# Kernel tuning notes

Measured on AMD Instinct MI355X. Metric: run time of the kernel, lower is better.

## Reference

```python
import jax, jax.numpy as jnp
import numpy as np
from jax import lax

H, P, N, G, K, CHUNK = 64, 64, 128, 1, 4, 256
D_MODEL = 2048
D_INNER = H * P            # 4096
CONV_DIM = D_INNER + 2 * G * N  # 4352
EPS = 1e-5


def setup_inputs() -> dict:
    key = jax.random.key(0)
    ks = jax.random.split(key, 6)
    s = lambda k, shape, scale: jax.random.normal(k, shape, jnp.float32) * scale
    return {
        "hidden_states": s(ks[0], (2, 2048, D_MODEL), 1.0),
        "in_proj_w": s(ks[1], (D_MODEL, D_INNER + CONV_DIM + H), D_MODEL ** -0.5),
        "conv_w": s(ks[2], (CONV_DIM, K), K ** -0.5),
        "conv_b": jnp.zeros((CONV_DIM,), jnp.float32),
        "dt_bias": jnp.ones((H,), jnp.float32),
        "A_log": jnp.log(jnp.arange(1, H + 1, dtype=jnp.float32)),
        "D_param": jnp.ones((H,), jnp.float32),
        "norm_w": jnp.ones((D_INNER,), jnp.float32),
        "out_proj_w": s(ks[3], (D_INNER, D_MODEL), D_INNER ** -0.5),
    }


def _mamba2_forward(hidden_states, in_proj_w, conv_w, conv_b, dt_bias, A_log, D_param, norm_w, out_proj_w):
    b, l, _ = hidden_states.shape
    c = l // CHUNK  # number of chunks

    # in_proj -> gate | conv channels (x,B,C) | dt
    proj = hidden_states @ in_proj_w
    gate = proj[..., :D_INNER]
    hbc = proj[..., D_INNER:D_INNER + CONV_DIM]
    dt = proj[..., D_INNER + CONV_DIM:]  # [b,l,H]

    # depthwise causal conv1d + silu
    xt = hbc.transpose(0, 2, 1)  # [b, CONV_DIM, l]
    y = lax.conv_general_dilated(
        xt, conv_w[:, None, :], window_strides=(1,), padding=[(K - 1, 0)],
        feature_group_count=CONV_DIM, dimension_numbers=("NCH", "OIH", "NCH"))
    hbc = jax.nn.silu(y + conv_b[None, :, None]).transpose(0, 2, 1)  # [b,l,CONV_DIM]

    # split into x / B / C per group (unflatten over groups as in torch code)
    per_g = D_INNER // G
    hg = hbc.reshape(b, l, G, per_g + 2 * N)
    x = hg[..., :per_g].reshape(b, l, H, P)                 # [b,l,h,p]
    Bm = hg[..., per_g:per_g + N]                            # [b,l,g,n]
    Cm = hg[..., per_g + N:]                                 # [b,l,g,n]
    hpg = H // G
    Bh = jnp.repeat(Bm, hpg, axis=2)                         # [b,l,h,n]
    Ch = jnp.repeat(Cm, hpg, axis=2)

    # dt: softplus(dt + bias), clamp per time_step_limit (0, inf)
    dt = jax.nn.softplus(dt + dt_bias)                       # [b,l,h]
    A = -jnp.exp(A_log)                                      # [h]

    # chunk the sequence
    x_c = x.reshape(b, c, CHUNK, H, P)
    B_c = Bh.reshape(b, c, CHUNK, H, N)
    C_c = Ch.reshape(b, c, CHUNK, H, N)
    dt_c = dt.reshape(b, c, CHUNK, H)

    dA = dt_c * A[None, None, None, :]                       # [b,c,L,h]
    cum = jnp.cumsum(dA, axis=2)                             # [b,c,L,h]

    # intra-chunk (diagonal block): decay[i,j] = exp(cum_i - cum_j), i>=j
    diff = cum[:, :, :, None, :] - cum[:, :, None, :, :]     # [b,c,i,j,h]
    i = jnp.arange(CHUNK)
    mask = i[:, None] >= i[None, :]
    decay = jnp.exp(jnp.where(mask[None, None, :, :, None], diff, -jnp.inf))
    scores = jnp.einsum("bcihn,bcjhn->bcijh", C_c, B_c) * decay * dt_c[:, :, None, :, :]
    Y_diag = jnp.einsum("bcijh,bcjhp->bcihp", scores, x_c)   # [b,c,L,h,p]

    # per-chunk final states
    decay_states = jnp.exp(cum[:, :, -1:, :] - cum)          # [b,c,L,h]
    states = jnp.einsum("bclh,bclhn,bclhp->bchpn", decay_states * dt_c, B_c, x_c)
    chunk_decay = jnp.exp(cum[:, :, -1, :])                  # [b,c,h]

    # inter-chunk recurrence over chunks
    def step(prev, inp):
        st, cd = inp  # [b,h,p,n], [b,h]
        new = cd[:, :, None, None] * prev + st
        return new, prev

    init = jnp.zeros((b, H, P, N), hidden_states.dtype)
    _, prev_states = lax.scan(step, init, (jnp.moveaxis(states, 1, 0), jnp.moveaxis(chunk_decay, 1, 0)))
    prev_states = jnp.moveaxis(prev_states, 0, 1)            # [b,c,h,p,n]

    state_decay_out = jnp.exp(cum)                           # [b,c,L,h]
    Y_off = jnp.einsum("bclhn,bchpn,bclh->bclhp", C_c, prev_states, state_decay_out)

    yh = (Y_diag + Y_off).reshape(b, l, H, P) + D_param[None, None, :, None] * x
    yr = yh.reshape(b, l, D_INNER)

    # gated RMSNorm
    hidden = yr * jax.nn.silu(gate)
    var = jnp.mean(hidden * hidden, axis=-1, keepdims=True)
    hidden = hidden * lax.rsqrt(var + EPS) * norm_w

    return hidden @ out_proj_w


def reference(hidden_states, in_proj_w, conv_w, conv_b, dt_bias, A_log, D_param, norm_w, out_proj_w):
    return _mamba2_forward(hidden_states, in_proj_w, conv_w, conv_b, dt_bias, A_log, D_param, norm_w, out_proj_w)
```

## Files before the change

kernel.cpp:

```cpp
#include <hip/hip_runtime.h>
#include <hip/hip_bf16.h>


typedef __attribute__((ext_vector_type(8))) _Float16 f16x8;
typedef __attribute__((ext_vector_type(4))) float f32x4;

#define GLD16(gp, lp) __builtin_amdgcn_global_load_lds( \
    (__attribute__((address_space(1))) void*)(gp),      \
    (__attribute__((address_space(3))) void*)(lp), 16, 0, 0)

__device__ __forceinline__ unsigned short f2h(float v) {
  _Float16 h = (_Float16)v;
  return *reinterpret_cast<unsigned short*>(&h);
}
__device__ __forceinline__ float h2f(unsigned short u) {
  _Float16 h = *reinterpret_cast<_Float16*>(&u);
  return (float)h;
}
__device__ __forceinline__ float siluf(float x) { return x / (1.f + expf(-x)); }

__global__ __launch_bounds__(256) void cast_f16(const float* __restrict__ s,
                                                _Float16* __restrict__ d) {
  long i = ((long)blockIdx.x * 256 + threadIdx.x) * 4;
  float4 v = *reinterpret_cast<const float4*>(s + i);
  ushort4 u;
  u.x = f2h(v.x); u.y = f2h(v.y); u.z = f2h(v.z); u.w = f2h(v.w);
  *reinterpret_cast<ushort4*>(d + i) = u;
}

__global__ __launch_bounds__(256) void transpose_win(const float* __restrict__ src,
                                                     _Float16* __restrict__ dst) {
  __shared__ float tile[32][33];
  int c0 = blockIdx.x * 32, r0 = blockIdx.y * 32;
  int tx = threadIdx.x, ty = threadIdx.y;
#pragma unroll
  for (int i = 0; i < 4; i++)
    tile[ty + i * 8][tx] = src[(long)(r0 + ty + i * 8) * 8512 + c0 + tx];
  __syncthreads();
#pragma unroll
  for (int i = 0; i < 4; i++) {
    int c = c0 + ty + i * 8, r = r0 + tx;
    dst[(long)c * 2048 + r] = (_Float16)tile[tx][ty + i * 8];
  }
}

__global__ __launch_bounds__(256) void transpose_wout(const float* __restrict__ src,
                                                      _Float16* __restrict__ dst,
                                                      int R, int C) {
  __shared__ float tile[32][33];
  int c0 = blockIdx.x * 32, r0 = blockIdx.y * 32;
  int tx = threadIdx.x, ty = threadIdx.y;
#pragma unroll
  for (int i = 0; i < 4; i++)
    tile[ty + i * 8][tx] = src[(long)(r0 + ty + i * 8) * C + c0 + tx];
  __syncthreads();
#pragma unroll
  for (int i = 0; i < 4; i++) {
    int c = c0 + ty + i * 8, r = r0 + tx;
    dst[(long)c * R + r] = (_Float16)tile[tx][ty + i * 8];
  }
}

__global__ __launch_bounds__(512, 2) void gemm_in8(const _Float16* __restrict__ A,
                                                   const _Float16* __restrict__ Bt,
                                                   _Float16* __restrict__ gate,
                                                   float* __restrict__ hbcf,
                                                   float* __restrict__ rparts) {
  __shared__ __attribute__((aligned(128))) char ldsB[131072];
  const int tid = threadIdx.x;
  const int lane = tid & 63;
  const int wv = tid >> 6;
  const int wr = wv >> 2, wc = wv & 3;
  const int wg = blockIdx.x;
  const bool rem = wg >= 512;
  int by, bxn, kbase, zz;
  if (!rem) {
    const int swz = (wg & 7) * 64 + (wg >> 3);
    by = swz >> 5; bxn = swz & 31; kbase = 0; zz = 0;
  } else {
    const int idx = wg - 512;
    by = idx & 15; zz = idx >> 4; bxn = 32; kbase = zz * 256;
  }

  const int srow = tid >> 3;
  const int scolg = (tid & 7) ^ (srow & 7);
  const _Float16* Ab = A + (long)by * 524288 + (long)srow * 2048 + scolg * 8 + kbase;
  const _Float16* Bb = Bt + (long)bxn * 524288 + (long)srow * 2048 + scolg * 8 + kbase;
  const int ldst = tid << 4;

#define STAGE_A(tau, h) do {                                              \
    const _Float16* g_ = Ab + (long)(h) * 262144 + (tau) * 64;            \
    char* l_ = ldsB + ((((tau) & 1) << 2) + (h)) * 16384 + ldst;          \
    GLD16(g_, l_); GLD16(g_ + 131072, l_ + 8192); } while (0)
#define STAGE_B(tau, h) do {                                              \
    const _Float16* g_ = Bb + (long)(h) * 262144 + (tau) * 64;            \
    char* l_ = ldsB + ((((tau) & 1) << 2) + 2 + (h)) * 16384 + ldst;      \
    GLD16(g_, l_); GLD16(g_ + 131072, l_ + 8192); } while (0)

  const int fr = lane & 15;
  const int c16 = (lane >> 4) ^ (fr & 7);
  const int aOff = wr * 16384 + fr * 128 + c16 * 16;
  const int bOff = (2 + (wc >> 1)) * 16384 + ((wc & 1) * 64 + fr) * 128 + c16 * 16;
#define RD_A(b, mi, k32) (*(const f16x8*)(ldsB + ((aOff + (b) * 65536 + (mi) * 2048) ^ ((k32) * 64))))
#define RD_B(b, ni, k32) (*(const f16x8*)(ldsB + ((bOff + (b) * 65536 + (ni) * 2048) ^ ((k32) * 64))))

#define BAR() __builtin_amdgcn_s_barrier()
#define WLG0() asm volatile("s_waitcnt lgkmcnt(0)" ::: "memory")
#define WLG8() asm volatile("s_waitcnt lgkmcnt(8)" ::: "memory")
#define WVM4() asm volatile("s_waitcnt vmcnt(4)" ::: "memory")

  f32x4 acc[8][4];
#pragma unroll
  for (int mi = 0; mi < 8; ++mi)
#pragma unroll
    for (int ni = 0; ni < 4; ++ni) acc[mi][ni] = f32x4{0.f, 0.f, 0.f, 0.f};

  STAGE_A(0, 0); STAGE_A(0, 1); STAGE_B(0, 0); STAGE_B(0, 1);
  STAGE_B(1, 0); STAGE_B(1, 1);
  WVM4(); BAR();

#define MFMA_Q(MI0, MI1, x0, x1, x2, x3, PB)                                        \
  __builtin_amdgcn_s_setprio(1);                                                    \
  _Pragma("unroll") for (int ni = 0; ni < 4; ++ni) {                                \
    acc[MI0][ni] = __builtin_amdgcn_mfma_f32_16x16x32_f16(x0, PB[ni][0], acc[MI0][ni], 0, 0, 0); \
    acc[MI0][ni] = __builtin_amdgcn_mfma_f32_16x16x32_f16(x1, PB[ni][1], acc[MI0][ni], 0, 0, 0); \
    acc[MI1][ni] = __builtin_amdgcn_mfma_f32_16x16x32_f16(x2, PB[ni][0], acc[MI1][ni], 0, 0, 0); \
    acc[MI1][ni] = __builtin_amdgcn_mfma_f32_16x16x32_f16(x3, PB[ni][1], acc[MI1][ni], 0, 0, 0); \
  }                                                                                 \
  __builtin_amdgcn_s_setprio(0);

#define ITER8(u, msk) do {                                                          \
    const int t1 = (2 * (u) + 1) & (msk);                                           \
    const int t2 = (2 * (u) + 2) & (msk);                                           \
    const int t3 = (2 * (u) + 3) & (msk);                                           \
    f16x8 PB0[4][2];                                                                \
    _Pragma("unroll") for (int ni = 0; ni < 4; ++ni) {                              \
      PB0[ni][0] = RD_B(0, ni, 0); PB0[ni][1] = RD_B(0, ni, 1); }                   \
    {                                                                               \
      f16x8 x0 = RD_A(0, 0, 0), x1 = RD_A(0, 0, 1), x2 = RD_A(0, 1, 0), x3 = RD_A(0, 1, 1); \
      STAGE_A(t1, 0); WLG8(); BAR(); WLG0();                                        \
      MFMA_Q(0, 1, x0, x1, x2, x3, PB0) BAR();                                      \
    }                                                                               \
    {                                                                               \
      f16x8 x0 = RD_A(0, 2, 0), x1 = RD_A(0, 2, 1), x2 = RD_A(0, 3, 0), x3 = RD_A(0, 3, 1); \
      STAGE_A(t1, 1); BAR(); WLG0();                                                \
      MFMA_Q(2, 3, x0, x1, x2, x3, PB0) BAR();                                      \
    }                                                                               \
    {                                                                               \
      f16x8 x0 = RD_A(0, 4, 0), x1 = RD_A(0, 4, 1), x2 = RD_A(0, 5, 0), x3 = RD_A(0, 5, 1); \
      STAGE_B(t2, 0); BAR(); WLG0();                                                \
      MFMA_Q(4, 5, x0, x1, x2, x3, PB0) BAR();                                      \
    }                                                                               \
    {                                                                               \
      f16x8 x0 = RD_A(0, 6, 0), x1 = RD_A(0, 6, 1), x2 = RD_A(0, 7, 0), x3 = RD_A(0, 7, 1); \
      STAGE_B(t2, 1); BAR(); WLG0();                                                \
      MFMA_Q(6, 7, x0, x1, x2, x3, PB0) WVM4(); BAR();                              \
    }                                                                               \
    f16x8 PB1[4][2];                                                                \
    _Pragma("unroll") for (int ni = 0; ni < 4; ++ni) {                              \
      PB1[ni][0] = RD_B(1, ni, 0); PB1[ni][1] = RD_B(1, ni, 1); }                   \
    {                                                                               \
      f16x8 x0 = RD_A(1, 0, 0), x1 = RD_A(1, 0, 1), x2 = RD_A(1, 1, 0), x3 = RD_A(1, 1, 1); \
      STAGE_A(t2, 0); WLG8(); BAR(); WLG0();                                        \
      MFMA_Q(0, 1, x0, x1, x2, x3, PB1) BAR();                                      \
    }                                                                               \
    {                                                                               \
      f16x8 x0 = RD_A(1, 2, 0), x1 = RD_A(1, 2, 1), x2 = RD_A(1, 3, 0), x3 = RD_A(1, 3, 1); \
      STAGE_A(t2, 1); BAR(); WLG0();                                                \
      MFMA_Q(2, 3, x0, x1, x2, x3, PB1) BAR();                                      \
    }                                                                               \
    {                                                                               \
      f16x8 x0 = RD_A(1, 4, 0), x1 = RD_A(1, 4, 1), x2 = RD_A(1, 5, 0), x3 = RD_A(1, 5, 1); \
      STAGE_B(t3, 0); BAR(); WLG0();                                                \
      MFMA_Q(4, 5, x0, x1, x2, x3, PB1) BAR();                                      \
    }                                                                               \
    {                                                                               \
      f16x8 x0 = RD_A(1, 6, 0), x1 = RD_A(1, 6, 1), x2 = RD_A(1, 7, 0), x3 = RD_A(1, 7, 1); \
      STAGE_B(t3, 1); BAR(); WLG0();                                                \
      MFMA_Q(6, 7, x0, x1, x2, x3, PB1) WVM4(); BAR();                              \
    }                                                                               \
  } while (0)

  if (!rem) {
    for (int u = 0; u < 16; ++u) ITER8(u, 31);
  } else {
    for (int u = 0; u < 2; ++u) ITER8(u, 3);
  }

  const int m0 = by * 256 + wr * 128;
  const int cl = lane & 15, rq = (lane >> 4) * 4;
  if (!rem) {
    const int n0 = bxn * 256 + wc * 64;
    if (bxn < 16) {
#pragma unroll
      for (int mi = 0; mi < 8; ++mi)
#pragma unroll
        for (int r = 0; r < 4; ++r) {
          long rowoff = (long)(m0 + mi * 16 + rq + r) * 4096 + n0 + cl;
#pragma unroll
          for (int ni = 0; ni < 4; ++ni) gate[rowoff + ni * 16] = (_Float16)acc[mi][ni][r];
        }
    } else {
#pragma unroll
      for (int mi = 0; mi < 8; ++mi)
#pragma unroll
        for (int r = 0; r < 4; ++r) {
          long rowoff = (long)(m0 + mi * 16 + rq + r) * 4352 + (n0 - 4096) + cl;
#pragma unroll
          for (int ni = 0; ni < 4; ++ni) hbcf[rowoff + ni * 16] = acc[mi][ni][r];
        }
    }
  } else {
    float* rp = rparts + (long)zz * 1048576;
    const int ncol = wc * 64;
#pragma unroll
    for (int mi = 0; mi < 8; ++mi)
#pragma unroll
      for (int r = 0; r < 4; ++r) {
        long rowoff = (long)(m0 + mi * 16 + rq + r) * 256 + ncol + cl;
#pragma unroll
        for (int ni = 0; ni < 4; ++ni) rp[rowoff + ni * 16] = acc[mi][ni][r];
      }
  }
#undef STAGE_A
#undef STAGE_B
#undef RD_A
#undef RD_B
#undef ITER8
}

__global__ __launch_bounds__(256) void add_rem(const float* __restrict__ rp,
                                               float* __restrict__ hbcf) {
  long e = ((long)blockIdx.x * 256 + threadIdx.x) * 4;
  float4 s = *reinterpret_cast<const float4*>(rp + e);
#pragma unroll
  for (int z = 1; z < 8; ++z) {
    float4 v = *reinterpret_cast<const float4*>(rp + (long)z * 1048576 + e);
    s.x += v.x; s.y += v.y; s.z += v.z; s.w += v.w;
  }
  long row = e >> 8, col = e & 255;
  *reinterpret_cast<float4*>(hbcf + row * 4352 + 4096 + col) = s;
}

__global__ __launch_bounds__(512, 2) void gemm_out8(const _Float16* __restrict__ A,
                                                    const _Float16* __restrict__ Bt,
                                                    float* __restrict__ Cp) {
  __shared__ __attribute__((aligned(128))) char ldsB[131072];
  const int tid = threadIdx.x;
  const int lane = tid & 63;
  const int wv = tid >> 6;
  const int wr = wv >> 2, wc = wv & 3;
  const int wg = blockIdx.x;
  const int z = wg >> 7;
  const int r7 = wg & 127;
  const int sw = (r7 & 7) * 16 + (r7 >> 3);
  const int by = sw >> 3, bx = sw & 7;

  const int srow = tid >> 3;
  const int scolg = (tid & 7) ^ (srow & 7);
  const _Float16* Ab = A + (long)by * 256 * 4096 + (long)z * 2048 +
                       (long)srow * 4096 + scolg * 8;
  const _Float16* Bb = Bt + (long)bx * 256 * 4096 + (long)z * 2048 +
                       (long)srow * 4096 + scolg * 8;
  const int ldst = tid << 4;

#define STAGE_A(tau, h) do {                                              \
    const _Float16* g_ = Ab + (long)(h) * 524288 + (tau) * 64;            \
    char* l_ = ldsB + ((((tau) & 1) << 2) + (h)) * 16384 + ldst;          \
    GLD16(g_, l_); GLD16(g_ + 262144, l_ + 8192); } while (0)
#define STAGE_B(tau, h) do {                                              \
    const _Float16* g_ = Bb + (long)(h) * 524288 + (tau) * 64;            \
    char* l_ = ldsB + ((((tau) & 1) << 2) + 2 + (h)) * 16384 + ldst;      \
    GLD16(g_, l_); GLD16(g_ + 262144, l_ + 8192); } while (0)

  const int fr = lane & 15;
  const int c16 = (lane >> 4) ^ (fr & 7);
  const int aOff = wr * 16384 + fr * 128 + c16 * 16;
  const int bOff = (2 + (wc >> 1)) * 16384 + ((wc & 1) * 64 + fr) * 128 + c16 * 16;
#define RD_A(b, mi, k32) (*(const f16x8*)(ldsB + ((aOff + (b) * 65536 + (mi) * 2048) ^ ((k32) * 64))))
#define RD_B(b, ni, k32) (*(const f16x8*)(ldsB + ((bOff + (b) * 65536 + (ni) * 2048) ^ ((k32) * 64))))

  f32x4 acc[8][4];
#pragma unroll
  for (int mi = 0; mi < 8; ++mi)
#pragma unroll
    for (int ni = 0; ni < 4; ++ni) acc[mi][ni] = f32x4{0.f, 0.f, 0.f, 0.f};

  STAGE_A(0, 0); STAGE_A(0, 1); STAGE_B(0, 0); STAGE_B(0, 1);
  STAGE_B(1, 0); STAGE_B(1, 1);
  WVM4(); BAR();

  for (int u = 0; u < 16; ++u) {
    const int t1 = 2 * u + 1;
    const int t2 = (2 * u + 2) & 31;
    const int t3 = (2 * u + 3) & 31;
    f16x8 PB0[4][2];
#pragma unroll
    for (int ni = 0; ni < 4; ++ni) { PB0[ni][0] = RD_B(0, ni, 0); PB0[ni][1] = RD_B(0, ni, 1); }
    {
      f16x8 x0 = RD_A(0, 0, 0), x1 = RD_A(0, 0, 1), x2 = RD_A(0, 1, 0), x3 = RD_A(0, 1, 1);
      STAGE_A(t1, 0); WLG8(); BAR(); WLG0();
      MFMA_Q(0, 1, x0, x1, x2, x3, PB0) BAR();
    }
    {
      f16x8 x0 = RD_A(0, 2, 0), x1 = RD_A(0, 2, 1), x2 = RD_A(0, 3, 0), x3 = RD_A(0, 3, 1);
      STAGE_A(t1, 1); BAR(); WLG0();
      MFMA_Q(2, 3, x0, x1, x2, x3, PB0) BAR();
    }
    {
      f16x8 x0 = RD_A(0, 4, 0), x1 = RD_A(0, 4, 1), x2 = RD_A(0, 5, 0), x3 = RD_A(0, 5, 1);
      STAGE_B(t2, 0); BAR(); WLG0();
      MFMA_Q(4, 5, x0, x1, x2, x3, PB0) BAR();
    }
    {
      f16x8 x0 = RD_A(0, 6, 0), x1 = RD_A(0, 6, 1), x2 = RD_A(0, 7, 0), x3 = RD_A(0, 7, 1);
      STAGE_B(t2, 1); BAR(); WLG0();
      MFMA_Q(6, 7, x0, x1, x2, x3, PB0) WVM4(); BAR();
    }
    f16x8 PB1[4][2];
#pragma unroll
    for (int ni = 0; ni < 4; ++ni) { PB1[ni][0] = RD_B(1, ni, 0); PB1[ni][1] = RD_B(1, ni, 1); }
    {
      f16x8 x0 = RD_A(1, 0, 0), x1 = RD_A(1, 0, 1), x2 = RD_A(1, 1, 0), x3 = RD_A(1, 1, 1);
      STAGE_A(t2, 0); WLG8(); BAR(); WLG0();
      MFMA_Q(0, 1, x0, x1, x2, x3, PB1) BAR();
    }
    {
      f16x8 x0 = RD_A(1, 2, 0), x1 = RD_A(1, 2, 1), x2 = RD_A(1, 3, 0), x3 = RD_A(1, 3, 1);
      STAGE_A(t2, 1); BAR(); WLG0();
      MFMA_Q(2, 3, x0, x1, x2, x3, PB1) BAR();
    }
    {
      f16x8 x0 = RD_A(1, 4, 0), x1 = RD_A(1, 4, 1), x2 = RD_A(1, 5, 0), x3 = RD_A(1, 5, 1);
      STAGE_B(t3, 0); BAR(); WLG0();
      MFMA_Q(4, 5, x0, x1, x2, x3, PB1) BAR();
    }
    {
      f16x8 x0 = RD_A(1, 6, 0), x1 = RD_A(1, 6, 1), x2 = RD_A(1, 7, 0), x3 = RD_A(1, 7, 1);
      STAGE_B(t3, 1); BAR(); WLG0();
      MFMA_Q(6, 7, x0, x1, x2, x3, PB1) WVM4(); BAR();
    }
  }
  const int m0 = by * 256 + wr * 128;
  const int n0 = bx * 256 + wc * 64;
  const int cl = lane & 15, rq = (lane >> 4) * 4;
  float* Cb = Cp + (long)z * 8388608;
#pragma unroll
  for (int mi = 0; mi < 8; ++mi)
#pragma unroll
    for (int r = 0; r < 4; ++r) {
      long rowoff = (long)(m0 + mi * 16 + rq + r) * 2048 + n0 + cl;
#pragma unroll
      for (int ni = 0; ni < 4; ++ni) Cb[rowoff + ni * 16] = acc[mi][ni][r];
    }
#undef STAGE_A
#undef STAGE_B
#undef RD_A
#undef RD_B
#undef BAR
#undef WLG0
#undef WLG8
#undef WVM4
#undef MFMA_Q
}

__global__ __launch_bounds__(256) void add_out(const float* __restrict__ p,
                                               float* __restrict__ o) {
  long i = ((long)blockIdx.x * 256 + threadIdx.x) * 4;
  float4 a = *reinterpret_cast<const float4*>(p + i);
  float4 b = *reinterpret_cast<const float4*>(p + 8388608 + i);
  float4 r;
  r.x = a.x + b.x; r.y = a.y + b.y; r.z = a.z + b.z; r.w = a.w + b.w;
  *reinterpret_cast<float4*>(o + i) = r;
}

__global__ __launch_bounds__(256) void gemm_bt(const _Float16* __restrict__ A,
                                               const _Float16* __restrict__ Bt,
                                               float* __restrict__ Cf,
                                               int K, int ldc,
                                               long zsA, long zsB, long zsC) {
  __shared__ uint4 As4[512];
  __shared__ uint4 Bs4[512];
  _Float16* As = (_Float16*)As4;
  _Float16* Bs = (_Float16*)Bs4;
  const int tid = threadIdx.x;
  const int wv = tid >> 6;
  const int lane = tid & 63;
  const _Float16* Ab = A + (long)blockIdx.z * zsA + (long)blockIdx.y * 128 * K;
  const _Float16* Bb = Bt + (long)blockIdx.z * zsB + (long)blockIdx.x * 128 * K;
  const int c0 = wv * 128 + lane;
  const int c1 = c0 + 64;
  const long ra0 = (long)(c0 >> 2) * K + (c0 & 3) * 8;
  const long ra1 = (long)(c1 >> 2) * K + (c1 & 3) * 8;
  f32x4 acc[4][4];
#pragma unroll
  for (int mi = 0; mi < 4; mi++)
#pragma unroll
    for (int ni = 0; ni < 4; ni++) acc[mi][ni] = f32x4{0.f, 0.f, 0.f, 0.f};
  const int mrow = (wv & 1) * 64 + (lane & 15);
  const int nrow = (wv >> 1) * 64 + (lane & 15);
  const int koff = (lane >> 4) * 8;
  for (int k0 = 0; k0 < K; k0 += 32) {
    GLD16(Ab + ra0 + k0, (char*)As + c0 * 16);
    GLD16(Ab + ra1 + k0, (char*)As + c1 * 16);
    GLD16(Bb + ra0 + k0, (char*)Bs + c0 * 16);
    GLD16(Bb + ra1 + k0, (char*)Bs + c1 * 16);
    __syncthreads();
    f16x8 af[4], bfr[4];
#pragma unroll
    for (int mi = 0; mi < 4; mi++)
      af[mi] = *(const f16x8*)(As + (mrow + mi * 16) * 32 + koff);
#pragma unroll
    for (int ni = 0; ni < 4; ni++)
      bfr[ni] = *(const f16x8*)(Bs + (nrow + ni * 16) * 32 + koff);
#pragma unroll
    for (int mi = 0; mi < 4; mi++)
#pragma unroll
      for (int ni = 0; ni < 4; ni++)
        acc[mi][ni] = __builtin_amdgcn_mfma_f32_16x16x32_f16(af[mi], bfr[ni],
                                                             acc[mi][ni], 0, 0, 0);
    __syncthreads();
  }
  const int m0 = blockIdx.y * 128 + (wv & 1) * 64;
  const int n0 = blockIdx.x * 128 + (wv >> 1) * 64;
  const int cl = lane & 15, rq = (lane >> 4) * 4;
  const long zc = (long)blockIdx.z * zsC;
#pragma unroll
  for (int mi = 0; mi < 4; mi++)
#pragma unroll
    for (int r = 0; r < 4; r++) {
      long rowoff = zc + (long)(m0 + mi * 16 + rq + r) * ldc + n0 + cl;
#pragma unroll
      for (int ni = 0; ni < 4; ni++) Cf[rowoff + ni * 16] = acc[mi][ni][r];
    }
}

__global__ __launch_bounds__(256) void dtz_kernel(const float* __restrict__ hs,
                                                  const float* __restrict__ Win,
                                                  float* __restrict__ zf) {
  __shared__ float Xs[4][2048];
  int t0 = blockIdx.x * 4;
  int tid = threadIdx.x;
#pragma unroll
  for (int i = 0; i < 8; i++) {
    int e = tid * 4 + i * 1024;
    int tok = e >> 11, k = e & 2047;
    *reinterpret_cast<float4*>(&Xs[tok][k]) =
        *reinterpret_cast<const float4*>(&hs[(long)(t0 + tok) * 2048 + k]);
  }
  __syncthreads();
  int h = tid & 63, tg = tid >> 6;
  float a0 = 0.f, a1 = 0.f, a2 = 0.f, a3 = 0.f;
  const float* wcol = Win + 8448 + h;
  for (int k = 0; k < 2048; k += 4) {
    a0 = fmaf(Xs[tg][k + 0], wcol[(long)(k + 0) * 8512], a0);
    a1 = fmaf(Xs[tg][k + 1], wcol[(long)(k + 1) * 8512], a1);
    a2 = fmaf(Xs[tg][k + 2], wcol[(long)(k + 2) * 8512], a2);
    a3 = fmaf(Xs[tg][k + 3], wcol[(long)(k + 3) * 8512], a3);
  }
  zf[(long)(t0 + tg) * 64 + h] = (a0 + a1) + (a2 + a3);
}

__global__ __launch_bounds__(256) void conv_silu_kernel(const float* __restrict__ hbcf,
                                                        const float* __restrict__ convw,
                                                        const float* __restrict__ convb,
                                                        _Float16* __restrict__ x16,
                                                        _Float16* __restrict__ B16,
                                                        _Float16* __restrict__ C16) {
  int q = blockIdx.x * 256 + threadIdx.x;
  int t = blockIdx.y;
  int l = t & 2047;
  const float* col = hbcf + (long)t * 4352 + q;
  float4 wq = *reinterpret_cast<const float4*>(convw + q * 4);
  float a = convb[q];
  if (l >= 3) a += col[-3 * 4352] * wq.x;
  if (l >= 2) a += col[-2 * 4352] * wq.y;
  if (l >= 1) a += col[-1 * 4352] * wq.z;
  a += col[0] * wq.w;
  _Float16 o = (_Float16)siluf(a);
  if (q < 4096) x16[(long)t * 4096 + q] = o;
  else if (q < 4224) B16[(long)t * 128 + (q - 4096)] = o;
  else C16[(long)t * 128 + (q - 4224)] = o;
}

__global__ __launch_bounds__(256) void xtrans(const unsigned short* __restrict__ src,
                                              unsigned short* __restrict__ dst) {
  __shared__ unsigned short tile[64][66];
  int c0 = blockIdx.x * 64, r0 = blockIdx.y * 64;
  int tx = threadIdx.x & 15, ty = threadIdx.x >> 4;
#pragma unroll
  for (int i = 0; i < 4; i++) {
    int r = ty + i * 16;
    ushort4 v = *(const ushort4*)&src[(long)(r0 + r) * 4096 + c0 + 4 * tx];
    tile[r][4 * tx] = v.x; tile[r][4 * tx + 1] = v.y;
    tile[r][4 * tx + 2] = v.z; tile[r][4 * tx + 3] = v.w;
  }
  __syncthreads();
#pragma unroll
  for (int i = 0; i < 4; i++) {
    int c = ty + i * 16;
    ushort4 v;
    v.x = tile[4 * tx + 0][c]; v.y = tile[4 * tx + 1][c];
    v.z = tile[4 * tx + 2][c]; v.w = tile[4 * tx + 3][c];
    *(ushort4*)&dst[(long)(c0 + c) * 4096 + r0 + 4 * tx] = v;
  }
}

__global__ __launch_bounds__(256) void dt_cum_kernel(const float* __restrict__ zf,
                                                     const float* __restrict__ dtb,
                                                     const float* __restrict__ Alog,
                                                     float* __restrict__ dt_f,
                                                     float* __restrict__ cum_f,
                                                     float* __restrict__ cuml) {
  int bc = blockIdx.x;
  int h = threadIdx.x & 63, seg = threadIdx.x >> 6;
  int t0 = bc * 256;
  float Ah = -expf(Alog[h]);
  float bias = dtb[h];
  __shared__ float segsum[4][64];
  float s = 0.f;
  for (int j = 0; j < 64; j++) {
    int t = t0 + seg * 64 + j;
    float z = zf[(long)t * 64 + h] + bias;
    float v = (z > 20.f) ? z : log1pf(expf(z));
    dt_f[(long)t * 64 + h] = v;
    s += v * Ah;
  }
  segsum[seg][h] = s;
  __syncthreads();
  float run = 0.f;
  for (int k = 0; k < seg; k++) run += segsum[k][h];
  for (int j = 0; j < 64; j++) {
    int t = t0 + seg * 64 + j;
    run += dt_f[(long)t * 64 + h] * Ah;
    cum_f[(long)t * 64 + h] = run;
  }
  if (seg == 3) cuml[bc * 64 + h] = run;
}

__global__ __launch_bounds__(256) void states_mfma(const unsigned short* __restrict__ xT16,
                                                   const unsigned short* __restrict__ B16,
                                                   const float* __restrict__ dt_f,
                                                   const float* __restrict__ cum_f,
                                                   const float* __restrict__ cuml,
                                                   float* __restrict__ states) {
  int h = blockIdx.x, bc = blockIdx.y;
  int t0 = bc * 256, tid = threadIdx.x;
  __shared__ float w_s[256];
  __shared__ unsigned short Aw[64 * 40];
  __shared__ unsigned short BT[128 * 40];
  {
    int t = t0 + tid;
    w_s[tid] = expf(cuml[bc * 64 + h] - cum_f[(long)t * 64 + h]) * dt_f[(long)t * 64 + h];
  }
  __syncthreads();
  int wv = tid >> 6, lane = tid & 63;
  int mr = lane & 15, koff = (lane >> 4) * 8;
  f32x4 acc[4][2];
#pragma unroll
  for (int mi = 0; mi < 4; mi++)
#pragma unroll
    for (int nj = 0; nj < 2; nj++) acc[mi][nj] = f32x4{0.f, 0.f, 0.f, 0.f};
  for (int kt = 0; kt < 8; kt++) {
    {
      int p = tid >> 2, tq = tid & 3;
      const unsigned short* g = &xT16[((long)(h * 64 + p)) * 4096 + t0 + kt * 32 + tq * 8];
      ushort4 u0 = *(const ushort4*)g, u1 = *(const ushort4*)(g + 4);
      const float* wp = &w_s[kt * 32 + tq * 8];
      ushort4 o0, o1;
      o0.x = f2h(h2f(u0.x) * wp[0]); o0.y = f2h(h2f(u0.y) * wp[1]);
      o0.z = f2h(h2f(u0.z) * wp[2]); o0.w = f2h(h2f(u0.w) * wp[3]);
      o1.x = f2h(h2f(u1.x) * wp[4]); o1.y = f2h(h2f(u1.y) * wp[5]);
      o1.z = f2h(h2f(u1.z) * wp[6]); o1.w = f2h(h2f(u1.w) * wp[7]);
      *(ushort4*)&Aw[p * 40 + tq * 8] = o0;
      *(ushort4*)&Aw[p * 40 + tq * 8 + 4] = o1;
    }
    {
      int tl = tid >> 3, ng = tid & 7;
      const unsigned short* g = &B16[((long)(t0 + kt * 32 + tl)) * 128 + ng * 16];
#pragma unroll
      for (int j = 0; j < 16; j++) BT[(ng * 16 + j) * 40 + tl] = g[j];
    }
    __syncthreads();
    f16x8 af[4], bf[2];
#pragma unroll
    for (int mi = 0; mi < 4; mi++)
      af[mi] = *(const f16x8*)&Aw[(mi * 16 + mr) * 40 + koff];
#pragma unroll
    for (int nj = 0; nj < 2; nj++)
      bf[nj] = *(const f16x8*)&BT[((wv * 2 + nj) * 16 + mr) * 40 + koff];
#pragma unroll
    for (int mi = 0; mi < 4; mi++)
#pragma unroll
      for (int nj = 0; nj < 2; nj++)
        acc[mi][nj] = __builtin_amdgcn_mfma_f32_16x16x32_f16(af[mi], bf[nj],
                                                             acc[mi][nj], 0, 0, 0);
    __syncthreads();
  }
  int cl = lane & 15, rq = (lane >> 4) * 4;
  long base = ((long)(bc * 64 + h)) * 8192;
#pragma unroll
  for (int mi = 0; mi < 4; mi++)
#pragma unroll
    for (int r = 0; r < 4; r++) {
      int p = mi * 16 + rq + r;
#pragma unroll
      for (int nj = 0; nj < 2; nj++) {
        int n = (wv * 2 + nj) * 16 + cl;
        states[base + p * 128 + n] = acc[mi][nj][r];
      }
    }
}

__global__ __launch_bounds__(256) void recur_kernel(float* __restrict__ states,
                                                    const float* __restrict__ cuml) {
  int bh = blockIdx.x;
  int b = bh >> 6, h = bh & 63;
  int tid = threadIdx.x;
  float4 prev[8];
#pragma unroll
  for (int j = 0; j < 8; j++) prev[j] = make_float4(0.f, 0.f, 0.f, 0.f);
  for (int c = 0; c < 8; c++) {
    int bc = b * 8 + c;
    float cd = expf(cuml[bc * 64 + h]);
    long base = (long)(bc * 64 + h) * 8192;
#pragma unroll
    for (int j = 0; j < 8; j++) {
      long o = base + j * 1024 + tid * 4;
      float4 st = *reinterpret_cast<const float4*>(&states[o]);
      *reinterpret_cast<float4*>(&states[o]) = prev[j];
      prev[j].x = fmaf(cd, prev[j].x, st.x);
      prev[j].y = fmaf(cd, prev[j].y, st.y);
      prev[j].z = fmaf(cd, prev[j].z, st.z);
      prev[j].w = fmaf(cd, prev[j].w, st.w);
    }
  }
}

__global__ __launch_bounds__(256) void yfused(const unsigned short* __restrict__ xT16,
                                              const unsigned short* __restrict__ x16,
                                              const unsigned short* __restrict__ C16,
                                              const float* __restrict__ CBT,
                                              const float* __restrict__ states,
                                              const float* __restrict__ dt_f,
                                              const float* __restrict__ cum_f,
                                              const float* __restrict__ Dp,
                                              float* __restrict__ Ysum) {
  int h = blockIdx.x, bc = blockIdx.y;
  int t0 = bc * 256, tid = threadIdx.x;
  __shared__ unsigned short Sb[256 * 40];
  __shared__ unsigned short Xb[64 * 264];
  __shared__ float cum_s[256], dt_s[256];
  int i = tid;
  cum_s[i] = cum_f[(long)(t0 + i) * 64 + h];
  dt_s[i] = dt_f[(long)(t0 + i) * 64 + h];
  {
    int p = tid >> 2, tq = tid & 3;
    const unsigned short* g = &xT16[((long)(h * 64 + p)) * 4096 + t0 + tq * 64];
    unsigned short* l = &Xb[p * 264 + tq * 64];
#pragma unroll
    for (int c = 0; c < 8; c++)
      *(uint4*)(l + c * 8) = *(const uint4*)(g + c * 8);
  }
  __syncthreads();
  float cum_i = cum_s[i];
  const float* cbrow = CBT + (long)bc * 65536 + (long)i * 256;
  int wv = tid >> 6, lane = tid & 63;
  int mr = lane & 15, koff = (lane >> 4) * 8;
  f32x4 acc[4][4];
#pragma unroll
  for (int mi = 0; mi < 4; mi++)
#pragma unroll
    for (int ni = 0; ni < 4; ni++) acc[mi][ni] = f32x4{0.f, 0.f, 0.f, 0.f};
  for (int kt = 0; kt < 8; kt++) {
    int k0 = kt * 32;
#pragma unroll
    for (int c = 0; c < 8; c++) {
      float4 cb = *(const float4*)&cbrow[k0 + c * 4];
      ushort4 o;
      {
        int j = k0 + c * 4 + 0;
        float s = (j <= i) ? cb.x * expf(cum_i - cum_s[j]) * dt_s[j] : 0.f;
        o.x = f2h(s);
      }
      {
        int j = k0 + c * 4 + 1;
        float s = (j <= i) ? cb.y * expf(cum_i - cum_s[j]) * dt_s[j] : 0.f;
        o.y = f2h(s);
      }
      {
        int j = k0 + c * 4 + 2;
        float s = (j <= i) ? cb.z * expf(cum_i - cum_s[j]) * dt_s[j] : 0.f;
        o.z = f2h(s);
      }
      {
        int j = k0 + c * 4 + 3;
        float s = (j <= i) ? cb.w * expf(cum_i - cum_s[j]) * dt_s[j] : 0.f;
        o.w = f2h(s);
      }
      *(ushort4*)&Sb[i * 40 + c * 4] = o;
    }
    __syncthreads();
    if (kt <= 2 * wv + 1) {
      f16x8 af[4], bf[4];
#pragma unroll
      for (int mi = 0; mi < 4; mi++)
        af[mi] = *(const f16x8*)&Sb[(64 * wv + mi * 16 + mr) * 40 + koff];
#pragma unroll
      for (int ni = 0; ni < 4; ni++)
        bf[ni] = *(const f16x8*)&Xb[(ni * 16 + mr) * 264 + k0 + koff];
#pragma unroll
      for (int mi = 0; mi < 4; mi++)
#pragma unroll
        for (int ni = 0; ni < 4; ni++)
          acc[mi][ni] = __builtin_amdgcn_mfma_f32_16x16x32_f16(af[mi], bf[ni],
                                                               acc[mi][ni], 0, 0, 0);
    }
    __syncthreads();
  }
  {
    int p = tid >> 2, nq = tid & 3;
    const float* g = &states[((long)(bc * 64 + h)) * 8192 + p * 128 + nq * 32];
    unsigned short* l = &Xb[p * 136 + nq * 32];
#pragma unroll
    for (int c = 0; c < 8; c++) {
      float4 v = *(const float4*)(g + c * 4);
      ushort4 u;
      u.x = f2h(v.x); u.y = f2h(v.y); u.z = f2h(v.z); u.w = f2h(v.w);
      *(ushort4*)(l + c * 4) = u;
    }
  }
  float fac_i = expf(cum_i);
  for (int kn = 0; kn < 4; kn++) {
    {
      const unsigned short* g = &C16[((long)(t0 + i)) * 128 + kn * 32];
#pragma unroll
      for (int c = 0; c < 8; c++) {
        ushort4 u = *(const ushort4*)(g + c * 4);
        ushort4 o;
        o.x = f2h(h2f(u.x) * fac_i); o.y = f2h(h2f(u.y) * fac_i);
        o.z = f2h(h2f(u.z) * fac_i); o.w = f2h(h2f(u.w) * fac_i);
        *(ushort4*)&Sb[i * 40 + c * 4] = o;
      }
    }
    __syncthreads();
    f16x8 af[4], bf[4];
#pragma unroll
    for (int mi = 0; mi < 4; mi++)
      af[mi] = *(const f16x8*)&Sb[(64 * wv + mi * 16 + mr) * 40 + koff];
#pragma unroll
    for (int ni = 0; ni < 4; ni++)
      bf[ni] = *(const f16x8*)&Xb[(ni * 16 + mr) * 136 + kn * 32 + koff];
#pragma unroll
    for (int mi = 0; mi < 4; mi++)
#pragma unroll
      for (int ni = 0; ni < 4; ni++)
        acc[mi][ni] = __builtin_amdgcn_mfma_f32_16x16x32_f16(af[mi], bf[ni],
                                                             acc[mi][ni], 0, 0, 0);
    __syncthreads();
  }
  float Dh = Dp[h];
  int cl = lane & 15, rq = (lane >> 4) * 4;
#pragma unroll
  for (int mi = 0; mi < 4; mi++)
#pragma unroll
    for (int r = 0; r < 4; r++) {
      long row = t0 + 64 * wv + mi * 16 + rq + r;
      float* yr = &Ysum[row * 4096 + h * 64];
      const unsigned short* xr = &x16[row * 4096 + h * 64];
#pragma unroll
      for (int ni = 0; ni < 4; ni++) {
        int p = ni * 16 + cl;
        yr[p] = acc[mi][ni][r] + Dh * h2f(xr[p]);
      }
    }
}

__global__ __launch_bounds__(256) void norm_kernel(const float* __restrict__ Ysum,
                                                   const _Float16* __restrict__ gate,
                                                   const float* __restrict__ nw,
                                                   _Float16* __restrict__ hid) {
  int t = blockIdx.x;
  int tid = threadIdx.x;
  float hv[16];
  float ss = 0.f;
#pragma unroll
  for (int k = 0; k < 4; k++) {
    int d = tid * 4 + k * 1024;
    float4 y = *reinterpret_cast<const float4*>(&Ysum[(long)t * 4096 + d]);
    ushort4 gu = *reinterpret_cast<const ushort4*>(gate + (long)t * 4096 + d);
    float h0 = y.x * siluf(h2f(gu.x)), h1 = y.y * siluf(h2f(gu.y));
    float h2 = y.z * siluf(h2f(gu.z)), h3 = y.w * siluf(h2f(gu.w));
    hv[k * 4 + 0] = h0; hv[k * 4 + 1] = h1; hv[k * 4 + 2] = h2; hv[k * 4 + 3] = h3;
    ss += h0 * h0 + h1 * h1 + h2 * h2 + h3 * h3;
  }
#pragma unroll
  for (int o = 32; o > 0; o >>= 1) ss += __shfl_down(ss, o, 64);
  __shared__ float ws4[4];
  if ((tid & 63) == 0) ws4[tid >> 6] = ss;
  __syncthreads();
  float var = (ws4[0] + ws4[1] + ws4[2] + ws4[3]) * (1.f / 4096.f);
  float scale = rsqrtf(var + 1e-5f);
#pragma unroll
  for (int k = 0; k < 4; k++) {
    int d = tid * 4 + k * 1024;
    ushort4 u;
#pragma unroll
    for (int c = 0; c < 4; c++)
      ((unsigned short*)&u)[c] = f2h(hv[k * 4 + c] * scale * nw[d + c]);
    *reinterpret_cast<ushort4*>(hid + (long)t * 4096 + d) = u;
  }
}

extern "C" void kernel_launch(void* const* d_in, const int* in_sizes, int n_in,
                              void* d_out, int out_size, void* d_ws, size_t ws_size,
                              hipStream_t stream) {
  (void)in_sizes; (void)n_in; (void)out_size; (void)ws_size;
  const float* hs    = (const float*)d_in[0];
  const float* Win   = (const float*)d_in[1];
  const float* convw = (const float*)d_in[2];
  const float* convb = (const float*)d_in[3];
  const float* dtb   = (const float*)d_in[4];
  const float* Alog  = (const float*)d_in[5];
  const float* Dp    = (const float*)d_in[6];
  const float* nw    = (const float*)d_in[7];
  const float* Wout  = (const float*)d_in[8];
  float* out = (float*)d_out;

  char* base = (char*)d_ws;
  size_t off = 0;
  auto take = [&](size_t n) { char* r = base + off; off += (n + 255) & ~(size_t)255; return r; };
  float*    hbcf  = (float*)take(4096UL * 4352 * 4);
  _Float16* gateh = (_Float16*)take(4096UL * 4096 * 2);
  _Float16* Ah    = (_Float16*)take(4096UL * 2048 * 2);
  _Float16* WtH   = (_Float16*)take(8448UL * 2048 * 2);
  _Float16* xT16  = (_Float16*)take(4096UL * 4096 * 2);
  _Float16* B16   = (_Float16*)take(4096UL * 128 * 2);
  _Float16* C16   = (_Float16*)take(4096UL * 128 * 2);
  float*    zf    = (float*)take(4096UL * 64 * 4);
  float*    dt_f  = (float*)take(4096UL * 64 * 4);
  float*    cum_f = (float*)take(4096UL * 64 * 4);
  float*    cuml  = (float*)take(16UL * 64 * 4);
  float*    CBT   = (float*)take(16UL * 256 * 256 * 4);
  float*    states= (float*)take(1024UL * 8192 * 4);
  float*    Ysum  = hbcf;
  float*    oparts= hbcf;
  float*    rparts= states;
  _Float16* WoutT = Ah;
  _Float16* x16   = WtH;
  _Float16* hid   = (_Float16*)states;

  dim3 tb(32, 8);
  cast_f16<<<8192, 256, 0, stream>>>(hs, Ah);
  transpose_win<<<dim3(264, 64), tb, 0, stream>>>(Win, WtH);
  dtz_kernel<<<1024, 256, 0, stream>>>(hs, Win, zf);
  gemm_in8<<<dim3(640), 512, 0, stream>>>(Ah, WtH, gateh, hbcf, rparts);
  add_rem<<<1024, 256, 0, stream>>>(rparts, hbcf);
  transpose_wout<<<dim3(64, 128), tb, 0, stream>>>(Wout, WoutT, 4096, 2048);
  conv_silu_kernel<<<dim3(17, 4096), 256, 0, stream>>>(hbcf, convw, convb, x16, B16, C16);
  dt_cum_kernel<<<16, 256, 0, stream>>>(zf, dtb, Alog, dt_f, cum_f, cuml);
  xtrans<<<dim3(64, 64), 256, 0, stream>>>((const unsigned short*)x16, (unsigned short*)xT16);
  gemm_bt<<<dim3(2, 2, 16), 256, 0, stream>>>(C16, B16, CBT, 128, 256,
                                              32768, 32768, 65536);
  states_mfma<<<dim3(64, 16), 256, 0, stream>>>((const unsigned short*)xT16,
                                                (const unsigned short*)B16,
                                                dt_f, cum_f, cuml, states);
  recur_kernel<<<128, 256, 0, stream>>>(states, cuml);
  yfused<<<dim3(64, 16), 256, 0, stream>>>((const unsigned short*)xT16,
                                           (const unsigned short*)x16,
                                           (const unsigned short*)C16,
                                           CBT, states, dt_f, cum_f, Dp, Ysum);
  norm_kernel<<<4096, 256, 0, stream>>>(Ysum, gateh, nw, hid);
  gemm_out8<<<dim3(256), 512, 0, stream>>>(hid, WoutT, oparts);
  add_out<<<8192, 256, 0, stream>>>(oparts, out);
}
```

Measured before the change: 777.3 us.

## Merge independent small kernels into multi-role launches and fuse conv with transpose

Independent preprocessing kernels are merged into single launches that branch on block index: cast, dt projection and W_in transpose become one prep kernel; dt cumsum, split-K reduction and W_out transpose become fuse2; the states and CB GEMMs become fuse3. The conv+silu kernel now also writes the transposed x tile directly, removing the separate xtrans pass. This cuts launch overhead and lets small tasks run concurrently, at the cost of heterogeneous blocks sharing one launch configuration and shared-memory size.

```diff
diff --git a/kernel.cpp b/kernel.cpp
--- a/kernel.cpp
+++ b/kernel.cpp
@@ -19,45 +19,55 @@
 }
 __device__ __forceinline__ float siluf(float x) { return x / (1.f + expf(-x)); }
 
-__global__ __launch_bounds__(256) void cast_f16(const float* __restrict__ s,
-                                                _Float16* __restrict__ d) {
-  long i = ((long)blockIdx.x * 256 + threadIdx.x) * 4;
-  float4 v = *reinterpret_cast<const float4*>(s + i);
-  ushort4 u;
-  u.x = f2h(v.x); u.y = f2h(v.y); u.z = f2h(v.z); u.w = f2h(v.w);
-  *reinterpret_cast<ushort4*>(d + i) = u;
-}
-
-__global__ __launch_bounds__(256) void transpose_win(const float* __restrict__ src,
-                                                     _Float16* __restrict__ dst) {
-  __shared__ float tile[32][33];
-  int c0 = blockIdx.x * 32, r0 = blockIdx.y * 32;
-  int tx = threadIdx.x, ty = threadIdx.y;
-#pragma unroll
-  for (int i = 0; i < 4; i++)
-    tile[ty + i * 8][tx] = src[(long)(r0 + ty + i * 8) * 8512 + c0 + tx];
-  __syncthreads();
-#pragma unroll
-  for (int i = 0; i < 4; i++) {
-    int c = c0 + ty + i * 8, r = r0 + tx;
-    dst[(long)c * 2048 + r] = (_Float16)tile[tx][ty + i * 8];
-  }
-}
-
-__global__ __launch_bounds__(256) void transpose_wout(const float* __restrict__ src,
-                                                      _Float16* __restrict__ dst,
-                                                      int R, int C) {
-  __shared__ float tile[32][33];
-  int c0 = blockIdx.x * 32, r0 = blockIdx.y * 32;
-  int tx = threadIdx.x, ty = threadIdx.y;
-#pragma unroll
-  for (int i = 0; i < 4; i++)
-    tile[ty + i * 8][tx] = src[(long)(r0 + ty + i * 8) * C + c0 + tx];
-  __syncthreads();
-#pragma unroll
-  for (int i = 0; i < 4; i++) {
-    int c = c0 + ty + i * 8, r = r0 + tx;
-    dst[(long)c * R + r] = (_Float16)tile[tx][ty + i * 8];
+__global__ __launch_bounds__(256) void prep(const float* __restrict__ hs,
+                                            const float* __restrict__ Win,
+                                            _Float16* __restrict__ Ah,
+                                            _Float16* __restrict__ WtH,
+                                            float* __restrict__ zf) {
+  __shared__ __attribute__((aligned(16))) char smemP[32768];
+  const int bid = blockIdx.x;
+  const int tid = threadIdx.x;
+  if (bid < 1024) {
+    float (*Xs)[2048] = reinterpret_cast<float (*)[2048]>(smemP);
+    int t0 = bid * 4;
+#pragma unroll
+    for (int i = 0; i < 8; i++) {
+      int e = tid * 4 + i * 1024;
+      int tok = e >> 11, k = e & 2047;
+      *reinterpret_cast<float4*>(&Xs[tok][k]) =
+          *reinterpret_cast<const float4*>(&hs[(long)(t0 + tok) * 2048 + k]);
+    }
+    __syncthreads();
+    int h = tid & 63, tg = tid >> 6;
+    float a0 = 0.f, a1 = 0.f, a2 = 0.f, a3 = 0.f;
+    const float* wcol = Win + 8448 + h;
+    for (int k = 0; k < 2048; k += 4) {
+      a0 = fmaf(Xs[tg][k + 0], wcol[(long)(k + 0) * 8512], a0);
+      a1 = fmaf(Xs[tg][k + 1], wcol[(long)(k + 1) * 8512], a1);
+      a2 = fmaf(Xs[tg][k + 2], wcol[(long)(k + 2) * 8512], a2);
+      a3 = fmaf(Xs[tg][k + 3], wcol[(long)(k + 3) * 8512], a3);
+    }
+    zf[(long)(t0 + tg) * 64 + h] = (a0 + a1) + (a2 + a3);
+  } else if (bid < 9216) {
+    long i = ((long)(bid - 1024) * 256 + tid) * 4;
+    float4 v = *reinterpret_cast<const float4*>(hs + i);
+    ushort4 u;
+    u.x = f2h(v.x); u.y = f2h(v.y); u.z = f2h(v.z); u.w = f2h(v.w);
+    *reinterpret_cast<ushort4*>((unsigned short*)Ah + i) = u;
+  } else {
+    float (*tile)[33] = reinterpret_cast<float (*)[33]>(smemP);
+    int i = bid - 9216;
+    int c0 = (i % 264) * 32, r0 = (i / 264) * 32;
+    int tx = tid & 31, ty = tid >> 5;
+#pragma unroll
+    for (int j = 0; j < 4; j++)
+      tile[ty + j * 8][tx] = Win[(long)(r0 + ty + j * 8) * 8512 + c0 + tx];
+    __syncthreads();
+#pragma unroll
+    for (int j = 0; j < 4; j++) {
+      int c = c0 + ty + j * 8, r = r0 + tx;
+      WtH[(long)c * 2048 + r] = (_Float16)tile[tx][ty + j * 8];
+    }
   }
 }
 
@@ -229,387 +239,258 @@
 #undef ITER8
 }
 
-__global__ __launch_bounds__(256) void add_rem(const float* __restrict__ rp,
-                                               float* __restrict__ hbcf) {
-  long e = ((long)blockIdx.x * 256 + threadIdx.x) * 4;
-  float4 s = *reinterpret_cast<const float4*>(rp + e);
-#pragma unroll
-  for (int z = 1; z < 8; ++z) {
-    float4 v = *reinterpret_cast<const float4*>(rp + (long)z * 1048576 + e);
-    s.x += v.x; s.y += v.y; s.z += v.z; s.w += v.w;
-  }
-  long row = e >> 8, col = e & 255;
-  *reinterpret_cast<float4*>(hbcf + row * 4352 + 4096 + col) = s;
-}
-
-__global__ __launch_bounds__(512, 2) void gemm_out8(const _Float16* __restrict__ A,
-                                                    const _Float16* __restrict__ Bt,
-                                                    float* __restrict__ Cp) {
-  __shared__ __attribute__((aligned(128))) char ldsB[131072];
+__global__ __launch_bounds__(256) void fuse2(const float* __restrict__ zf,
+                                             const float* __restrict__ dtb,
+                                             const float* __restrict__ Alog,
+                                             float* __restrict__ dt_f,
+                                             float* __restrict__ cum_f,
+                                             float* __restrict__ cuml,
+                                             const float* __restrict__ rp,
+                                             float* __restrict__ hbcf,
+                                             const float* __restrict__ Wout,
+                                             _Float16* __restrict__ WoutT) {
+  __shared__ __attribute__((aligned(16))) char smem2[4352];
+  const int bid = blockIdx.x;
   const int tid = threadIdx.x;
-  const int lane = tid & 63;
-  const int wv = tid >> 6;
-  const int wr = wv >> 2, wc = wv & 3;
-  const int wg = blockIdx.x;
-  const int z = wg >> 7;
-  const int r7 = wg & 127;
-  const int sw = (r7 & 7) * 16 + (r7 >> 3);
-  const int by = sw >> 3, bx = sw & 7;
-
-  const int srow = tid >> 3;
-  const int scolg = (tid & 7) ^ (srow & 7);
-  const _Float16* Ab = A + (long)by * 256 * 4096 + (long)z * 2048 +
-                       (long)srow * 4096 + scolg * 8;
-  const _Float16* Bb = Bt + (long)bx * 256 * 4096 + (long)z * 2048 +
-                       (long)srow * 4096 + scolg * 8;
-  const int ldst = tid << 4;
-
-#define STAGE_A(tau, h) do {                                              \
-    const _Float16* g_ = Ab + (long)(h) * 524288 + (tau) * 64;            \
-    char* l_ = ldsB + ((((tau) & 1) << 2) + (h)) * 16384 + ldst;          \
-    GLD16(g_, l_); GLD16(g_ + 262144, l_ + 8192); } while (0)
-#define STAGE_B(tau, h) do {                                              \
-    const _Float16* g_ = Bb + (long)(h) * 524288 + (tau) * 64;            \
-    char* l_ = ldsB + ((((tau) & 1) << 2) + 2 + (h)) * 16384 + ldst;      \
-    GLD16(g_, l_); GLD16(g_ + 262144, l_ + 8192); } while (0)
-
-  const int fr = lane & 15;
-  const int c16 = (lane >> 4) ^ (fr & 7);
-  const int aOff = wr * 16384 + fr * 128 + c16 * 16;
-  const int bOff = (2 + (wc >> 1)) * 16384 + ((wc & 1) * 64 + fr) * 128 + c16 * 16;
-#define RD_A(b, mi, k32) (*(const f16x8*)(ldsB + ((aOff + (b) * 65536 + (mi) * 2048) ^ ((k32) * 64))))
-#define RD_B(b, ni, k32) (*(const f16x8*)(ldsB + ((bOff + (b) * 65536 + (ni) * 2048) ^ ((k32) * 64))))
-
-  f32x4 acc[8][4];
-#pragma unroll
-  for (int mi = 0; mi < 8; ++mi)
-#pragma unroll
-    for (int ni = 0; ni < 4; ++ni) acc[mi][ni] = f32x4{0.f, 0.f, 0.f, 0.f};
-
-  STAGE_A(0, 0); STAGE_A(0, 1); STAGE_B(0, 0); STAGE_B(0, 1);
-  STAGE_B(1, 0); STAGE_B(1, 1);
-  WVM4(); BAR();
-
-  for (int u = 0; u < 16; ++u) {
-    const int t1 = 2 * u + 1;
-    const int t2 = (2 * u + 2) & 31;
-    const int t3 = (2 * u + 3) & 31;
-    f16x8 PB0[4][2];
-#pragma unroll
-    for (int ni = 0; ni < 4; ++ni) { PB0[ni][0] = RD_B(0, ni, 0); PB0[ni][1] = RD_B(0, ni, 1); }
-    {
-      f16x8 x0 = RD_A(0, 0, 0), x1 = RD_A(0, 0, 1), x2 = RD_A(0, 1, 0), x3 = RD_A(0, 1, 1);
-      STAGE_A(t1, 0); WLG8(); BAR(); WLG0();
-      MFMA_Q(0, 1, x0, x1, x2, x3, PB0) BAR();
-    }
-    {
-      f16x8 x0 = RD_A(0, 2, 0), x1 = RD_A(0, 2, 1), x2 = RD_A(0, 3, 0), x3 = RD_A(0, 3, 1);
-      STAGE_A(t1, 1); BAR(); WLG0();
-      MFMA_Q(2, 3, x0, x1, x2, x3, PB0) BAR();
-    }
-    {
-      f16x8 x0 = RD_A(0, 4, 0), x1 = RD_A(0, 4, 1), x2 = RD_A(0, 5, 0), x3 = RD_A(0, 5, 1);
-      STAGE_B(t2, 0); BAR(); WLG0();
-      MFMA_Q(4, 5, x0, x1, x2, x3, PB0) BAR();
-    }
-    {
-      f16x8 x0 = RD_A(0, 6, 0), x1 = RD_A(0, 6, 1), x2 = RD_A(0, 7, 0), x3 = RD_A(0, 7, 1);
-      STAGE_B(t2, 1); BAR(); WLG0();
-      MFMA_Q(6, 7, x0, x1, x2, x3, PB0) WVM4(); BAR();
-    }
-    f16x8 PB1[4][2];
-#pragma unroll
-    for (int ni = 0; ni < 4; ++ni) { PB1[ni][0] = RD_B(1, ni, 0); PB1[ni][1] = RD_B(1, ni, 1); }
-    {
-      f16x8 x0 = RD_A(1, 0, 0), x1 = RD_A(1, 0, 1), x2 = RD_A(1, 1, 0), x3 = RD_A(1, 1, 1);
-      STAGE_A(t2, 0); WLG8(); BAR(); WLG0();
-      MFMA_Q(0, 1, x0, x1, x2, x3, PB1) BAR();
-    }
-    {
-      f16x8 x0 = RD_A(1, 2, 0), x1 = RD_A(1, 2, 1), x2 = RD_A(1, 3, 0), x3 = RD_A(1, 3, 1);
-      STAGE_A(t2, 1); BAR(); WLG0();
-      MFMA_Q(2, 3, x0, x1, x2, x3, PB1) BAR();
-    }
-    {
-      f16x8 x0 = RD_A(1, 4, 0), x1 = RD_A(1, 4, 1), x2 = RD_A(1, 5, 0), x3 = RD_A(1, 5, 1);
-      STAGE_B(t3, 0); BAR(); WLG0();
-      MFMA_Q(4, 5, x0, x1, x2, x3, PB1) BAR();
-    }
-    {
-      f16x8 x0 = RD_A(1, 6, 0), x1 = RD_A(1, 6, 1), x2 = RD_A(1, 7, 0), x3 = RD_A(1, 7, 1);
-      STAGE_B(t3, 1); BAR(); WLG0();
-      MFMA_Q(6, 7, x0, x1, x2, x3, PB1) WVM4(); BAR();
-    }
-  }
-  const int m0 = by * 256 + wr * 128;
-  const int n0 = bx * 256 + wc * 64;
-  const int cl = lane & 15, rq = (lane >> 4) * 4;
-  float* Cb = Cp + (long)z * 8388608;
-#pragma unroll
-  for (int mi = 0; mi < 8; ++mi)
-#pragma unroll
-    for (int r = 0; r < 4; ++r) {
-      long rowoff = (long)(m0 + mi * 16 + rq + r) * 2048 + n0 + cl;
-#pragma unroll
-      for (int ni = 0; ni < 4; ++ni) Cb[rowoff + ni * 16] = acc[mi][ni][r];
-    }
-#undef STAGE_A
-#undef STAGE_B
-#undef RD_A
-#undef RD_B
-#undef BAR
-#undef WLG0
-#undef WLG8
-#undef WVM4
-#undef MFMA_Q
-}
-
-__global__ __launch_bounds__(256) void add_out(const float* __restrict__ p,
-                                               float* __restrict__ o) {
-  long i = ((long)blockIdx.x * 256 + threadIdx.x) * 4;
-  float4 a = *reinterpret_cast<const float4*>(p + i);
-  float4 b = *reinterpret_cast<const float4*>(p + 8388608 + i);
-  float4 r;
-  r.x = a.x + b.x; r.y = a.y + b.y; r.z = a.z + b.z; r.w = a.w + b.w;
-  *reinterpret_cast<float4*>(o + i) = r;
-}
-
-__global__ __launch_bounds__(256) void gemm_bt(const _Float16* __restrict__ A,
-                                               const _Float16* __restrict__ Bt,
-                                               float* __restrict__ Cf,
-                                               int K, int ldc,
-                                               long zsA, long zsB, long zsC) {
-  __shared__ uint4 As4[512];
-  __shared__ uint4 Bs4[512];
-  _Float16* As = (_Float16*)As4;
-  _Float16* Bs = (_Float16*)Bs4;
+  if (bid < 16) {
+    float (*segsum)[64] = reinterpret_cast<float (*)[64]>(smem2);
+    int bc = bid;
+    int h = tid & 63, seg = tid >> 6;
+    int t0 = bc * 256;
+    float Ah = -expf(Alog[h]);
+    float bias = dtb[h];
+    float s = 0.f;
+    for (int j = 0; j < 64; j++) {
+      int t = t0 + seg * 64 + j;
+      float z = zf[(long)t * 64 + h] + bias;
+      float v = (z > 20.f) ? z : log1pf(expf(z));
+      dt_f[(long)t * 64 + h] = v;
+      s += v * Ah;
+    }
+    segsum[seg][h] = s;
+    __syncthreads();
+    float run = 0.f;
+    for (int k = 0; k < seg; k++) run += segsum[k][h];
+    for (int j = 0; j < 64; j++) {
+      int t = t0 + seg * 64 + j;
+      run += dt_f[(long)t * 64 + h] * Ah;
+      cum_f[(long)t * 64 + h] = run;
+    }
+    if (seg == 3) cuml[bc * 64 + h] = run;
+  } else if (bid < 1040) {
+    long e = ((long)(bid - 16) * 256 + tid) * 4;
+    float4 s = *reinterpret_cast<const float4*>(rp + e);
+#pragma unroll
+    for (int z = 1; z < 8; ++z) {
+      float4 v = *reinterpret_cast<const float4*>(rp + (long)z * 1048576 + e);
+      s.x += v.x; s.y += v.y; s.z += v.z; s.w += v.w;
+    }
+    long row = e >> 8, col = e & 255;
+    *reinterpret_cast<float4*>(hbcf + row * 4352 + 4096 + col) = s;
+  } else {
+    float (*tile)[33] = reinterpret_cast<float (*)[33]>(smem2);
+    int i = bid - 1040;
+    int c0 = (i & 63) * 32, r0 = (i >> 6) * 32;
+    int tx = tid & 31, ty = tid >> 5;
+#pragma unroll
+    for (int j = 0; j < 4; j++)
+      tile[ty + j * 8][tx] = Wout[(long)(r0 + ty + j * 8) * 2048 + c0 + tx];
+    __syncthreads();
+#pragma unroll
+    for (int j = 0; j < 4; j++) {
+      int c = c0 + ty + j * 8, r = r0 + tx;
+      WoutT[(long)c * 4096 + r] = (_Float16)tile[tx][ty + j * 8];
+    }
+  }
+}
+
+__global__ __launch_bounds__(256) void convx(const float* __restrict__ hbcf,
+                                             const float* __restrict__ convw,
+                                             const float* __restrict__ convb,
+                                             _Float16* __restrict__ x16,
+                                             _Float16* __restrict__ B16,
+                                             _Float16* __restrict__ C16,
+                                             unsigned short* __restrict__ xT16) {
+  __shared__ unsigned short tile[64][66];
+  const int bx = blockIdx.x, t0 = blockIdx.y * 64;
   const int tid = threadIdx.x;
-  const int wv = tid >> 6;
-  const int lane = tid & 63;
-  const _Float16* Ab = A + (long)blockIdx.z * zsA + (long)blockIdx.y * 128 * K;
-  const _Float16* Bb = Bt + (long)blockIdx.z * zsB + (long)blockIdx.x * 128 * K;
-  const int c0 = wv * 128 + lane;
-  const int c1 = c0 + 64;
-  const long ra0 = (long)(c0 >> 2) * K + (c0 & 3) * 8;
-  const long ra1 = (long)(c1 >> 2) * K + (c1 & 3) * 8;
-  f32x4 acc[4][4];
-#pragma unroll
-  for (int mi = 0; mi < 4; mi++)
-#pragma unroll
-    for (int ni = 0; ni < 4; ni++) acc[mi][ni] = f32x4{0.f, 0.f, 0.f, 0.f};
-  const int mrow = (wv & 1) * 64 + (lane & 15);
-  const int nrow = (wv >> 1) * 64 + (lane & 15);
-  const int koff = (lane >> 4) * 8;
-  for (int k0 = 0; k0 < K; k0 += 32) {
-    GLD16(Ab + ra0 + k0, (char*)As + c0 * 16);
-    GLD16(Ab + ra1 + k0, (char*)As + c1 * 16);
-    GLD16(Bb + ra0 + k0, (char*)Bs + c0 * 16);
-    GLD16(Bb + ra1 + k0, (char*)Bs + c1 * 16);
-    __syncthreads();
-    f16x8 af[4], bfr[4];
+  const int tq = tid & 63, tg = tid >> 6;
+  const int q0 = (bx < 64) ? bx * 64 : 4096 + (bx - 64) * 64;
+  const int q = q0 + tq;
+  const int ts = t0 + tg * 16;
+  const int bstart = ts & ~2047;
+  const float* colq = hbcf + q;
+  float4 wq = *reinterpret_cast<const float4*>(convw + q * 4);
+  float bconv = convb[q];
+  float v3 = (ts - 3 >= bstart) ? colq[(long)(ts - 3) * 4352] : 0.f;
+  float v2 = (ts - 2 >= bstart) ? colq[(long)(ts - 2) * 4352] : 0.f;
+  float v1 = (ts - 1 >= bstart) ? colq[(long)(ts - 1) * 4352] : 0.f;
+  if (bx < 64) {
+#pragma unroll
+    for (int j = 0; j < 16; ++j) {
+      int t = ts + j;
+      float v0 = colq[(long)t * 4352];
+      float a = bconv + v3 * wq.x + v2 * wq.y + v1 * wq.z + v0 * wq.w;
+      unsigned short o = f2h(siluf(a));
+      ((unsigned short*)x16)[(long)t * 4096 + q] = o;
+      tile[tg * 16 + j][tq] = o;
+      v3 = v2; v2 = v1; v1 = v0;
+    }
+    __syncthreads();
+    int tx = tid & 15, ty = tid >> 4;
+#pragma unroll
+    for (int i = 0; i < 4; ++i) {
+      int c = ty + i * 16;
+      ushort4 v;
+      v.x = tile[4 * tx + 0][c]; v.y = tile[4 * tx + 1][c];
+      v.z = tile[4 * tx + 2][c]; v.w = tile[4 * tx + 3][c];
+      *(ushort4*)&xT16[(long)(q0 + c) * 4096 + t0 + 4 * tx] = v;
+    }
+  } else {
+#pragma unroll
+    for (int j = 0; j < 16; ++j) {
+      int t = ts + j;
+      float v0 = colq[(long)t * 4352];
+      float a = bconv + v3 * wq.x + v2 * wq.y + v1 * wq.z + v0 * wq.w;
+      _Float16 o = (_Float16)siluf(a);
+      if (q < 4224) B16[(long)t * 128 + (q - 4096)] = o;
+      else C16[(long)t * 128 + (q - 4224)] = o;
+      v3 = v2; v2 = v1; v1 = v0;
+    }
+  }
+}
+
+__global__ __launch_bounds__(256) void fuse3(const unsigned short* __restrict__ xT16,
+                                             const _Float16* __restrict__ B16,
+                                             const _Float16* __restrict__ C16,
+                                             const float* __restrict__ dt_f,
+                                             const float* __restrict__ cum_f,
+                                             const float* __restrict__ cuml,
+                                             float* __restrict__ states,
+                                             float* __restrict__ CBT) {
+  __shared__ __attribute__((aligned(16))) char smem3[16384];
+  const int bid = blockIdx.x;
+  const int tid = threadIdx.x;
+  const int wv = tid >> 6, lane = tid & 63;
+  const int mr = lane & 15, koff = (lane >> 4) * 8;
+  if (bid < 1024) {
+    float* w_s = (float*)smem3;
+    unsigned short* Aw = (unsigned short*)(smem3 + 1024);
+    unsigned short* BT = (unsigned short*)(smem3 + 6144);
+    int h = bid & 63, bc = bid >> 6;
+    int t0 = bc * 256;
+    {
+      int t = t0 + tid;
+      w_s[tid] = expf(cuml[bc * 64 + h] - cum_f[(long)t * 64 + h]) * dt_f[(long)t * 64 + h];
+    }
+    __syncthreads();
+    f32x4 acc[4][2];
 #pragma unroll
     for (int mi = 0; mi < 4; mi++)
-      af[mi] = *(const f16x8*)(As + (mrow + mi * 16) * 32 + koff);
-#pragma unroll
-    for (int ni = 0; ni < 4; ni++)
-      bfr[ni] = *(const f16x8*)(Bs + (nrow + ni * 16) * 32 + koff);
+#pragma unroll
+      for (int nj = 0; nj < 2; nj++) acc[mi][nj] = f32x4{0.f, 0.f, 0.f, 0.f};
+    for (int kt = 0; kt < 8; kt++) {
+      {
+        int p = tid >> 2, tq2 = tid & 3;
+        const unsigned short* g = &xT16[((long)(h * 64 + p)) * 4096 + t0 + kt * 32 + tq2 * 8];
+        ushort4 u0 = *(const ushort4*)g, u1 = *(const ushort4*)(g + 4);
+        const float* wp = &w_s[kt * 32 + tq2 * 8];
+        ushort4 o0, o1;
+        o0.x = f2h(h2f(u0.x) * wp[0]); o0.y = f2h(h2f(u0.y) * wp[1]);
+        o0.z = f2h(h2f(u0.z) * wp[2]); o0.w = f2h(h2f(u0.w) * wp[3]);
+        o1.x = f2h(h2f(u1.x) * wp[4]); o1.y = f2h(h2f(u1.y) * wp[5]);
+        o1.z = f2h(h2f(u1.z) * wp[6]); o1.w = f2h(h2f(u1.w) * wp[7]);
+        *(ushort4*)&Aw[p * 40 + tq2 * 8] = o0;
+        *(ushort4*)&Aw[p * 40 + tq2 * 8 + 4] = o1;
+      }
+      {
+        int tl = tid >> 3, ng = tid & 7;
+        const unsigned short* g = (const unsigned short*)B16 +
+                                  ((long)(t0 + kt * 32 + tl)) * 128 + ng * 16;
+#pragma unroll
+        for (int j = 0; j < 16; j++) BT[(ng * 16 + j) * 40 + tl] = g[j];
+      }
+      __syncthreads();
+      f16x8 af[4], bf[2];
+#pragma unroll
+      for (int mi = 0; mi < 4; mi++)
+        af[mi] = *(const f16x8*)&Aw[(mi * 16 + mr) * 40 + koff];
+#pragma unroll
+      for (int nj = 0; nj < 2; nj++)
+        bf[nj] = *(const f16x8*)&BT[((wv * 2 + nj) * 16 + mr) * 40 + koff];
+#pragma unroll
+      for (int mi = 0; mi < 4; mi++)
+#pragma unroll
+        for (int nj = 0; nj < 2; nj++)
+          acc[mi][nj] = __builtin_amdgcn_mfma_f32_16x16x32_f16(af[mi], bf[nj],
+                                                               acc[mi][nj], 0, 0, 0);
+      __syncthreads();
+    }
+    int cl = lane & 15, rq = (lane >> 4) * 4;
+    long base = ((long)(bc * 64 + h)) * 8192;
 #pragma unroll
     for (int mi = 0; mi < 4; mi++)
 #pragma unroll
+      for (int r = 0; r < 4; r++) {
+        int p = mi * 16 + rq + r;
+#pragma unroll
+        for (int nj = 0; nj < 2; nj++) {
+          int n = (wv * 2 + nj) * 16 + cl;
+          states[base + p * 128 + n] = acc[mi][nj][r];
+        }
+      }
+  } else {
+    _Float16* As = (_Float16*)smem3;
+    _Float16* Bs = (_Float16*)(smem3 + 8192);
+    int i = bid - 1024;
+    int bx = i & 1, by = (i >> 1) & 1, bz = i >> 2;
+    const _Float16* Ab = C16 + (long)bz * 32768 + (long)by * 128 * 128;
+    const _Float16* Bb = B16 + (long)bz * 32768 + (long)bx * 128 * 128;
+    const int c0 = wv * 128 + lane;
+    const int c1 = c0 + 64;
+    const long ra0 = (long)(c0 >> 2) * 128 + (c0 & 3) * 8;
+    const long ra1 = (long)(c1 >> 2) * 128 + (c1 & 3) * 8;
+    f32x4 acc[4][4];
+#pragma unroll
+    for (int mi = 0; mi < 4; mi++)
+#pragma unroll
+      for (int ni = 0; ni < 4; ni++) acc[mi][ni] = f32x4{0.f, 0.f, 0.f, 0.f};
+    const int mrow = (wv & 1) * 64 + (lane & 15);
+    const int nrow = (wv >> 1) * 64 + (lane & 15);
+    for (int k0 = 0; k0 < 128; k0 += 32) {
+      GLD16(Ab + ra0 + k0, (char*)As + c0 * 16);
+      GLD16(Ab + ra1 + k0, (char*)As + c1 * 16);
+      GLD16(Bb + ra0 + k0, (char*)Bs + c0 * 16);
+      GLD16(Bb + ra1 + k0, (char*)Bs + c1 * 16);
+      __syncthreads();
+      f16x8 af[4], bfr[4];
+#pragma unroll
+      for (int mi = 0; mi < 4; mi++)
+        af[mi] = *(const f16x8*)(As + (mrow + mi * 16) * 32 + koff);
+#pragma unroll
       for (int ni = 0; ni < 4; ni++)
-        acc[mi][ni] = __builtin_amdgcn_mfma_f32_16x16x32_f16(af[mi], bfr[ni],
-                                                             acc[mi][ni], 0, 0, 0);
-    __syncthreads();
-  }
-  const int m0 = blockIdx.y * 128 + (wv & 1) * 64;
-  const int n0 = blockIdx.x * 128 + (wv >> 1) * 64;
-  const int cl = lane & 15, rq = (lane >> 4) * 4;
-  const long zc = (long)blockIdx.z * zsC;
-#pragma unroll
-  for (int mi = 0; mi < 4; mi++)
-#pragma unroll
-    for (int r = 0; r < 4; r++) {
-      long rowoff = zc + (long)(m0 + mi * 16 + rq + r) * ldc + n0 + cl;
-#pragma unroll
-      for (int ni = 0; ni < 4; ni++) Cf[rowoff + ni * 16] = acc[mi][ni][r];
-    }
-}
-
-__global__ __launch_bounds__(256) void dtz_kernel(const float* __restrict__ hs,
-                                                  const float* __restrict__ Win,
-                                                  float* __restrict__ zf) {
-  __shared__ float Xs[4][2048];
-  int t0 = blockIdx.x * 4;
-  int tid = threadIdx.x;
-#pragma unroll
-  for (int i = 0; i < 8; i++) {
-    int e = tid * 4 + i * 1024;
-    int tok = e >> 11, k = e & 2047;
-    *reinterpret_cast<float4*>(&Xs[tok][k]) =
-        *reinterpret_cast<const float4*>(&hs[(long)(t0 + tok) * 2048 + k]);
-  }
-  __syncthreads();
-  int h = tid & 63, tg = tid >> 6;
-  float a0 = 0.f, a1 = 0.f, a2 = 0.f, a3 = 0.f;
-  const float* wcol = Win + 8448 + h;
-  for (int k = 0; k < 2048; k += 4) {
-    a0 = fmaf(Xs[tg][k + 0], wcol[(long)(k + 0) * 8512], a0);
-    a1 = fmaf(Xs[tg][k + 1], wcol[(long)(k + 1) * 8512], a1);
-    a2 = fmaf(Xs[tg][k + 2], wcol[(long)(k + 2) * 8512], a2);
-    a3 = fmaf(Xs[tg][k + 3], wcol[(long)(k + 3) * 8512], a3);
-  }
-  zf[(long)(t0 + tg) * 64 + h] = (a0 + a1) + (a2 + a3);
-}
-
-__global__ __launch_bounds__(256) void conv_silu_kernel(const float* __restrict__ hbcf,
-                                                        const float* __restrict__ convw,
-                                                        const float* __restrict__ convb,
-                                                        _Float16* __restrict__ x16,
-                                                        _Float16* __restrict__ B16,
-                                                        _Float16* __restrict__ C16) {
-  int q = blockIdx.x * 256 + threadIdx.x;
-  int t = blockIdx.y;
-  int l = t & 2047;
-  const float* col = hbcf + (long)t * 4352 + q;
-  float4 wq = *reinterpret_cast<const float4*>(convw + q * 4);
-  float a = convb[q];
-  if (l >= 3) a += col[-3 * 4352] * wq.x;
-  if (l >= 2) a += col[-2 * 4352] * wq.y;
-  if (l >= 1) a += col[-1 * 4352] * wq.z;
-  a += col[0] * wq.w;
-  _Float16 o = (_Float16)siluf(a);
-  if (q < 4096) x16[(long)t * 4096 + q] = o;
-  else if (q < 4224) B16[(long)t * 128 + (q - 4096)] = o;
-  else C16[(long)t * 128 + (q - 4224)] = o;
-}
-
-__global__ __launch_bounds__(256) void xtrans(const unsigned short* __restrict__ src,
-                                              unsigned short* __restrict__ dst) {
-  __shared__ unsigned short tile[64][66];
-  int c0 = blockIdx.x * 64, r0 = blockIdx.y * 64;
-  int tx = threadIdx.x & 15, ty = threadIdx.x >> 4;
-#pragma unroll
-  for (int i = 0; i < 4; i++) {
-    int r = ty + i * 16;
-    ushort4 v = *(const ushort4*)&src[(long)(r0 + r) * 4096 + c0 + 4 * tx];
-    tile[r][4 * tx] = v.x; tile[r][4 * tx + 1] = v.y;
-    tile[r][4 * tx + 2] = v.z; tile[r][4 * tx + 3] = v.w;
-  }
-  __syncthreads();
-#pragma unroll
-  for (int i = 0; i < 4; i++) {
-    int c = ty + i * 16;
-    ushort4 v;
-    v.x = tile[4 * tx + 0][c]; v.y = tile[4 * tx + 1][c];
-    v.z = tile[4 * tx + 2][c]; v.w = tile[4 * tx + 3][c];
-    *(ushort4*)&dst[(long)(c0 + c) * 4096 + r0 + 4 * tx] = v;
-  }
-}
-
-__global__ __launch_bounds__(256) void dt_cum_kernel(const float* __restrict__ zf,
-                                                     const float* __restrict__ dtb,
-                                                     const float* __restrict__ Alog,
-                                                     float* __restrict__ dt_f,
-                                                     float* __restrict__ cum_f,
-                                                     float* __restrict__ cuml) {
-  int bc = blockIdx.x;
-  int h = threadIdx.x & 63, seg = threadIdx.x >> 6;
-  int t0 = bc * 256;
-  float Ah = -expf(Alog[h]);
-  float bias = dtb[h];
-  __shared__ float segsum[4][64];
-  float s = 0.f;
-  for (int j = 0; j < 64; j++) {
-    int t = t0 + seg * 64 + j;
-    float z = zf[(long)t * 64 + h] + bias;
-    float v = (z > 20.f) ? z : log1pf(expf(z));
-    dt_f[(long)t * 64 + h] = v;
-    s += v * Ah;
-  }
-  segsum[seg][h] = s;
-  __syncthreads();
-  float run = 0.f;
-  for (int k = 0; k < seg; k++) run += segsum[k][h];
-  for (int j = 0; j < 64; j++) {
-    int t = t0 + seg * 64 + j;
-    run += dt_f[(long)t * 64 + h] * Ah;
-    cum_f[(long)t * 64 + h] = run;
-  }
-  if (seg == 3) cuml[bc * 64 + h] = run;
-}
-
-__global__ __launch_bounds__(256) void states_mfma(const unsigned short* __restrict__ xT16,
-                                                   const unsigned short* __restrict__ B16,
-                                                   const float* __restrict__ dt_f,
-                                                   const float* __restrict__ cum_f,
-                                                   const float* __restrict__ cuml,
-                                                   float* __restrict__ states) {
-  int h = blockIdx.x, bc = blockIdx.y;
-  int t0 = bc * 256, tid = threadIdx.x;
-  __shared__ float w_s[256];
-  __shared__ unsigned short Aw[64 * 40];
-  __shared__ unsigned short BT[128 * 40];
-  {
-    int t = t0 + tid;
-    w_s[tid] = expf(cuml[bc * 64 + h] - cum_f[(long)t * 64 + h]) * dt_f[(long)t * 64 + h];
-  }
-  __syncthreads();
-  int wv = tid >> 6, lane = tid & 63;
-  int mr = lane & 15, koff = (lane >> 4) * 8;
-  f32x4 acc[4][2];
-#pragma unroll
-  for (int mi = 0; mi < 4; mi++)
-#pragma unroll
-    for (int nj = 0; nj < 2; nj++) acc[mi][nj] = f32x4{0.f, 0.f, 0.f, 0.f};
-  for (int kt = 0; kt < 8; kt++) {
-    {
-      int p = tid >> 2, tq = tid & 3;
-      const unsigned short* g = &xT16[((long)(h * 64 + p)) * 4096 + t0 + kt * 32 + tq * 8];
-      ushort4 u0 = *(const ushort4*)g, u1 = *(const ushort4*)(g + 4);
-      const float* wp = &w_s[kt * 32 + tq * 8];
-      ushort4 o0, o1;
-      o0.x = f2h(h2f(u0.x) * wp[0]); o0.y = f2h(h2f(u0.y) * wp[1]);
-      o0.z = f2h(h2f(u0.z) * wp[2]); o0.w = f2h(h2f(u0.w) * wp[3]);
-      o1.x = f2h(h2f(u1.x) * wp[4]); o1.y = f2h(h2f(u1.y) * wp[5]);
-      o1.z = f2h(h2f(u1.z) * wp[6]); o1.w = f2h(h2f(u1.w) * wp[7]);
-      *(ushort4*)&Aw[p * 40 + tq * 8] = o0;
-      *(ushort4*)&Aw[p * 40 + tq * 8 + 4] = o1;
-    }
-    {
-      int tl = tid >> 3, ng = tid & 7;
-      const unsigned short* g = &B16[((long)(t0 + kt * 32 + tl)) * 128 + ng * 16];
-#pragma unroll
-      for (int j = 0; j < 16; j++) BT[(ng * 16 + j) * 40 + tl] = g[j];
-    }
-    __syncthreads();
-    f16x8 af[4], bf[2];
+        bfr[ni] = *(const f16x8*)(Bs + (nrow + ni * 16) * 32 + koff);
+#pragma unroll
+      for (int mi = 0; mi < 4; mi++)
+#pragma unroll
+        for (int ni = 0; ni < 4; ni++)
+          acc[mi][ni] = __builtin_amdgcn_mfma_f32_16x16x32_f16(af[mi], bfr[ni],
+                                                               acc[mi][ni], 0, 0, 0);
+      __syncthreads();
+    }
+    const int m0 = by * 128 + (wv & 1) * 64;
+    const int n0 = bx * 128 + (wv >> 1) * 64;
+    const int cl = lane & 15, rq = (lane >> 4) * 4;
+    const long zc = (long)bz * 65536;
 #pragma unroll
     for (int mi = 0; mi < 4; mi++)
-      af[mi] = *(const f16x8*)&Aw[(mi * 16 + mr) * 40 + koff];
-#pragma unroll
-    for (int nj = 0; nj < 2; nj++)
-      bf[nj] = *(const f16x8*)&BT[((wv * 2 + nj) * 16 + mr) * 40 + koff];
-#pragma unroll
-    for (int mi = 0; mi < 4; mi++)
-#pragma unroll
-      for (int nj = 0; nj < 2; nj++)
-        acc[mi][nj] = __builtin_amdgcn_mfma_f32_16x16x32_f16(af[mi], bf[nj],
-                                                             acc[mi][nj], 0, 0, 0);
-    __syncthreads();
-  }
-  int cl = lane & 15, rq = (lane >> 4) * 4;
-  long base = ((long)(bc * 64 + h)) * 8192;
-#pragma unroll
-  for (int mi = 0; mi < 4; mi++)
-#pragma unroll
-    for (int r = 0; r < 4; r++) {
-      int p = mi * 16 + rq + r;
-#pragma unroll
-      for (int nj = 0; nj < 2; nj++) {
-        int n = (wv * 2 + nj) * 16 + cl;
-        states[base + p * 128 + n] = acc[mi][nj][r];
-      }
-    }
+#pragma unroll
+      for (int r = 0; r < 4; r++) {
+        long rowoff = zc + (long)(m0 + mi * 16 + rq + r) * 256 + n0 + cl;
+#pragma unroll
+        for (int ni = 0; ni < 4; ni++) CBT[rowoff + ni * 16] = acc[mi][ni][r];
+      }
+  }
 }
 
 __global__ __launch_bounds__(256) void recur_kernel(float* __restrict__ states,
@@ -810,6 +691,138 @@
       ((unsigned short*)&u)[c] = f2h(hv[k * 4 + c] * scale * nw[d + c]);
     *reinterpret_cast<ushort4*>(hid + (long)t * 4096 + d) = u;
   }
+}
+
+__global__ __launch_bounds__(512, 2) void gemm_out8(const _Float16* __restrict__ A,
+                                                    const _Float16* __restrict__ Bt,
+                                                    float* __restrict__ Cp) {
+  __shared__ __attribute__((aligned(128))) char ldsB[131072];
+  const int tid = threadIdx.x;
+  const int lane = tid & 63;
+  const int wv = tid >> 6;
+  const int wr = wv >> 2, wc = wv & 3;
+  const int wg = blockIdx.x;
+  const int z = wg >> 7;
+  const int r7 = wg & 127;
+  const int sw = (r7 & 7) * 16 + (r7 >> 3);
+  const int by = sw >> 3, bx = sw & 7;
+
+  const int srow = tid >> 3;
+  const int scolg = (tid & 7) ^ (srow & 7);
+  const _Float16* Ab = A + (long)by * 256 * 4096 + (long)z * 2048 +
+                       (long)srow * 4096 + scolg * 8;
+  const _Float16* Bb = Bt + (long)bx * 256 * 4096 + (long)z * 2048 +
+                       (long)srow * 4096 + scolg * 8;
+  const int ldst = tid << 4;
+
+#define STAGE_A(tau, h) do {                                              \
+    const _Float16* g_ = Ab + (long)(h) * 524288 + (tau) * 64;            \
+    char* l_ = ldsB + ((((tau) & 1) << 2) + (h)) * 16384 + ldst;          \
+    GLD16(g_, l_); GLD16(g_ + 262144, l_ + 8192); } while (0)
+#define STAGE_B(tau, h) do {                                              \
+    const _Float16* g_ = Bb + (long)(h) * 524288 + (tau) * 64;            \
+    char* l_ = ldsB + ((((tau) & 1) << 2) + 2 + (h)) * 16384 + ldst;      \
+    GLD16(g_, l_); GLD16(g_ + 262144, l_ + 8192); } while (0)
+
+  const int fr = lane & 15;
+  const int c16 = (lane >> 4) ^ (fr & 7);
+  const int aOff = wr * 16384 + fr * 128 + c16 * 16;
+  const int bOff = (2 + (wc >> 1)) * 16384 + ((wc & 1) * 64 + fr) * 128 + c16 * 16;
+#define RD_A(b, mi, k32) (*(const f16x8*)(ldsB + ((aOff + (b) * 65536 + (mi) * 2048) ^ ((k32) * 64))))
+#define RD_B(b, ni, k32) (*(const f16x8*)(ldsB + ((bOff + (b) * 65536 + (ni) * 2048) ^ ((k32) * 64))))
+
+  f32x4 acc[8][4];
+#pragma unroll
+  for (int mi = 0; mi < 8; ++mi)
+#pragma unroll
+    for (int ni = 0; ni < 4; ++ni) acc[mi][ni] = f32x4{0.f, 0.f, 0.f, 0.f};
+
+  STAGE_A(0, 0); STAGE_A(0, 1); STAGE_B(0, 0); STAGE_B(0, 1);
+  STAGE_B(1, 0); STAGE_B(1, 1);
+  WVM4(); BAR();
+
+  for (int u = 0; u < 16; ++u) {
+    const int t1 = 2 * u + 1;
+    const int t2 = (2 * u + 2) & 31;
+    const int t3 = (2 * u + 3) & 31;
+    f16x8 PB0[4][2];
+#pragma unroll
+    for (int ni = 0; ni < 4; ++ni) { PB0[ni][0] = RD_B(0, ni, 0); PB0[ni][1] = RD_B(0, ni, 1); }
+    {
+      f16x8 x0 = RD_A(0, 0, 0), x1 = RD_A(0, 0, 1), x2 = RD_A(0, 1, 0), x3 = RD_A(0, 1, 1);
+      STAGE_A(t1, 0); WLG8(); BAR(); WLG0();
+      MFMA_Q(0, 1, x0, x1, x2, x3, PB0) BAR();
+    }
+    {
+      f16x8 x0 = RD_A(0, 2, 0), x1 = RD_A(0, 2, 1), x2 = RD_A(0, 3, 0), x3 = RD_A(0, 3, 1);
+      STAGE_A(t1, 1); BAR(); WLG0();
+      MFMA_Q(2, 3, x0, x1, x2, x3, PB0) BAR();
+    }
+    {
+      f16x8 x0 = RD_A(0, 4, 0), x1 = RD_A(0, 4, 1), x2 = RD_A(0, 5, 0), x3 = RD_A(0, 5, 1);
+      STAGE_B(t2, 0); BAR(); WLG0();
+      MFMA_Q(4, 5, x0, x1, x2, x3, PB0) BAR();
+    }
+    {
+      f16x8 x0 = RD_A(0, 6, 0), x1 = RD_A(0, 6, 1), x2 = RD_A(0, 7, 0), x3 = RD_A(0, 7, 1);
+      STAGE_B(t2, 1); BAR(); WLG0();
+      MFMA_Q(6, 7, x0, x1, x2, x3, PB0) WVM4(); BAR();
+    }
+    f16x8 PB1[4][2];
+#pragma unroll
+    for (int ni = 0; ni < 4; ++ni) { PB1[ni][0] = RD_B(1, ni, 0); PB1[ni][1] = RD_B(1, ni, 1); }
+    {
+      f16x8 x0 = RD_A(1, 0, 0), x1 = RD_A(1, 0, 1), x2 = RD_A(1, 1, 0), x3 = RD_A(1, 1, 1);
+      STAGE_A(t2, 0); WLG8(); BAR(); WLG0();
+      MFMA_Q(0, 1, x0, x1, x2, x3, PB1) BAR();
+    }
+    {
+      f16x8 x0 = RD_A(1, 2, 0), x1 = RD_A(1, 2, 1), x2 = RD_A(1, 3, 0), x3 = RD_A(1, 3, 1);
+      STAGE_A(t2, 1); BAR(); WLG0();
+      MFMA_Q(2, 3, x0, x1, x2, x3, PB1) BAR();
+    }
+    {
+      f16x8 x0 = RD_A(1, 4, 0), x1 = RD_A(1, 4, 1), x2 = RD_A(1, 5, 0), x3 = RD_A(1, 5, 1);
+      STAGE_B(t3, 0); BAR(); WLG0();
+      MFMA_Q(4, 5, x0, x1, x2, x3, PB1) BAR();
+    }
+    {
+      f16x8 x0 = RD_A(1, 6, 0), x1 = RD_A(1, 6, 1), x2 = RD_A(1, 7, 0), x3 = RD_A(1, 7, 1);
+      STAGE_B(t3, 1); BAR(); WLG0();
+      MFMA_Q(6, 7, x0, x1, x2, x3, PB1) WVM4(); BAR();
+    }
+  }
+  const int m0 = by * 256 + wr * 128;
+  const int n0 = bx * 256 + wc * 64;
+  const int cl = lane & 15, rq = (lane >> 4) * 4;
+  float* Cb = Cp + (long)z * 8388608;
+#pragma unroll
+  for (int mi = 0; mi < 8; ++mi)
+#pragma unroll
+    for (int r = 0; r < 4; ++r) {
+      long rowoff = (long)(m0 + mi * 16 + rq + r) * 2048 + n0 + cl;
+#pragma unroll
+      for (int ni = 0; ni < 4; ++ni) Cb[rowoff + ni * 16] = acc[mi][ni][r];
+    }
+#undef STAGE_A
+#undef STAGE_B
+#undef RD_A
+#undef RD_B
+#undef BAR
+#undef WLG0
+#undef WLG8
+#undef WVM4
+#undef MFMA_Q
+}
+
+__global__ __launch_bounds__(256) void add_out(const float* __restrict__ p,
+                                               float* __restrict__ o) {
+  long i = ((long)blockIdx.x * 256 + threadIdx.x) * 4;
+  float4 a = *reinterpret_cast<const float4*>(p + i);
+  float4 b = *reinterpret_cast<const float4*>(p + 8388608 + i);
+  float4 r;
+  r.x = a.x + b.x; r.y = a.y + b.y; r.z = a.z + b.z; r.w = a.w + b.w;
+  *reinterpret_cast<float4*>(o + i) = r;
 }
 
 extern "C" void kernel_launch(void* const* d_in, const int* in_sizes, int n_in,
@@ -850,21 +863,14 @@
   _Float16* x16   = WtH;
   _Float16* hid   = (_Float16*)states;
 
-  dim3 tb(32, 8);
-  cast_f16<<<8192, 256, 0, stream>>>(hs, Ah);
-  transpose_win<<<dim3(264, 64), tb, 0, stream>>>(Win, WtH);
-  dtz_kernel<<<1024, 256, 0, stream>>>(hs, Win, zf);
+  prep<<<26112, 256, 0, stream>>>(hs, Win, Ah, WtH, zf);
   gemm_in8<<<dim3(640), 512, 0, stream>>>(Ah, WtH, gateh, hbcf, rparts);
-  add_rem<<<1024, 256, 0, stream>>>(rparts, hbcf);
-  transpose_wout<<<dim3(64, 128), tb, 0, stream>>>(Wout, WoutT, 4096, 2048);
-  conv_silu_kernel<<<dim3(17, 4096), 256, 0, stream>>>(hbcf, convw, convb, x16, B16, C16);
-  dt_cum_kernel<<<16, 256, 0, stream>>>(zf, dtb, Alog, dt_f, cum_f, cuml);
-  xtrans<<<dim3(64, 64), 256, 0, stream>>>((const unsigned short*)x16, (unsigned short*)xT16);
-  gemm_bt<<<dim3(2, 2, 16), 256, 0, stream>>>(C16, B16, CBT, 128, 256,
-                                              32768, 32768, 65536);
-  states_mfma<<<dim3(64, 16), 256, 0, stream>>>((const unsigned short*)xT16,
-                                                (const unsigned short*)B16,
-                                                dt_f, cum_f, cuml, states);
+  fuse2<<<9232, 256, 0, stream>>>(zf, dtb, Alog, dt_f, cum_f, cuml,
+                                  rparts, hbcf, Wout, WoutT);
+  convx<<<dim3(68, 64), 256, 0, stream>>>(hbcf, convw, convb, x16, B16, C16,
+                                          (unsigned short*)xT16);
+  fuse3<<<1088, 256, 0, stream>>>((const unsigned short*)xT16, B16, C16,
+                                  dt_f, cum_f, cuml, states, CBT);
   recur_kernel<<<128, 256, 0, stream>>>(states, cuml);
   yfused<<<dim3(64, 16), 256, 0, stream>>>((const unsigned short*)xT16,
                                            (const unsigned short*)x16,
```

New measurement: 714.1 us. -8.1%, faster.
